# Performance work log

Measured on AMD Instinct MI355X. Metric: run time of the kernel, lower is better.

The kernel has to match this reference:

```python
import jax, jax.numpy as jnp
import numpy as np

B, S = 8, 128
D_SENS, D_ACT, D_STR, D_ENC, DIM = 512, 32, 128, 128, 128
D_JOINT = D_STR + D_ENC  # 256


def _l2norm(x):
    return x / jnp.clip(jnp.linalg.norm(x, axis=-1, keepdims=True), 1e-12)


def _mlp(x, layers):
    # layers: list of (W, b); ReLU between layers, none on output
    n = len(layers)
    for i, (W, b) in enumerate(layers):
        x = x @ W + b
        if i < n - 1:
            x = jax.nn.relu(x)
    return x


def _meta_mlp(x, p):
    x = jax.nn.relu(x @ p['W1'] + p['b1'])
    x = jax.nn.relu(x @ p['W2'] + p['b2'])
    return x @ p['W3'] + p['b3']


def setup_inputs() -> dict:
    key = jax.random.key(0)
    it = iter(jax.random.split(key, 40))
    w = lambda shape, s=0.02: jax.random.normal(next(it), shape, jnp.float32) * s
    H = D_ACT * 4  # to_transitions hidden dim (default mlp_hidden_dim)
    return dict(
        sensory=jax.random.normal(next(it), (B, S, D_SENS), jnp.float32),
        actions=jax.random.normal(next(it), (B, S, D_ACT), jnp.float32),
        init_hidden=w((1, D_STR), 0.01),
        tW1=w((D_ACT, H)), tb1=w((H,)),
        tW2=w((H, H)), tb2=w((H,)),
        tW3=w((H, D_STR * D_STR)), tb3=w((D_STR * D_STR,)),
        enc_w=w((D_SENS, D_ENC)), enc_b=w((D_ENC,)),
        dec_w=w((D_ENC, D_SENS)), dec_b=w((D_SENS,)),
        q_w=w((D_JOINT, DIM)), k_w=w((D_JOINT, DIM)), v_w=w((D_JOINT, DIM)),
        mW1=w((DIM, 2 * DIM)), mb1=w((2 * DIM,)),
        mW2=w((2 * DIM, 2 * DIM)), mb2=w((2 * DIM,)),
        mW3=w((2 * DIM, DIM)), mb3=w((DIM,)),
        oW1=w((DIM, 2 * DIM)), ob1=w((2 * DIM,)),
        oW2=w((2 * DIM, 2 * DIM)), ob2=w((2 * DIM,)),
        oW3=w((2 * DIM, D_JOINT)), ob3=w((D_JOINT,)),
        sW1=w((2 * D_STR + 1, 2 * D_STR)), sb1=w((2 * D_STR,)),
        sW2=w((2 * D_STR, 2 * D_STR)), sb2=w((2 * D_STR,)),
        sW3=w((2 * D_STR, D_STR)), sb3=w((D_STR,)),
        integration_ratio=jnp.asarray(0.1, jnp.float32),
    )


def reference(sensory, actions, init_hidden, tW1, tb1, tW2, tb2, tW3, tb3,
              enc_w, enc_b, dec_w, dec_b, q_w, k_w, v_w,
              mW1, mb1, mW2, mb2, mW3, mb3,
              oW1, ob1, oW2, ob2, oW3, ob3,
              sW1, sb1, sW2, sb2, sW3, sb3, integration_ratio):
    mse = lambda a, b: jnp.mean((a - b) ** 2)

    # --- PathIntegration: actions -> transitions -> scripted RNN scan ---
    trans = _mlp(actions, [(tW1, tb1), (tW2, tb2), (tW3, tb3)])  # (B,S,ds*ds)
    trans = trans.reshape(B, S, D_STR, D_STR)
    h0 = jnp.broadcast_to(_l2norm(init_hidden), (B, D_STR))

    def step(h, T):  # h (B,ds), T (B,ds,ds)
        h = _l2norm(jax.nn.relu(jnp.einsum('bi,bij->bj', h, T)))
        return h, h

    _, hs = jax.lax.scan(step, h0, jnp.swapaxes(trans, 0, 1))
    structural = jnp.swapaxes(hs, 0, 1)  # (B,S,ds)

    # --- sensory encoder (Linear) ---
    encoded = sensory @ enc_w + enc_b  # (B,S,D_ENC)

    meta_params = {'W1': mW1, 'b1': mb1, 'W2': mW2, 'b2': mb2, 'W3': mW3, 'b3': mb3}

    def retrieve(s, e):
        joint = jnp.concatenate((s, e), axis=-1)
        q = joint @ q_w
        r = _meta_mlp(q, meta_params)
        out = _mlp(r, [(oW1, ob1), (oW2, ob2), (oW3, ob3)])
        return out[..., :D_STR], out[..., D_STR:]

    # generative branch
    dec_gen_s, dec_enc = retrieve(structural, jnp.zeros_like(encoded))
    generative_pred_loss = mse(sensory, dec_enc @ dec_w + dec_b)

    # relational branch (source calls retrieve(zeros, encoded) twice)
    dec_s1, _ = retrieve(jnp.zeros_like(structural), encoded)
    dec_s2, _ = retrieve(jnp.zeros_like(structural), encoded)
    relational_loss = mse(dec_s1, structural) + mse(dec_s2, structural)

    # consistency / inference correction
    corr_s, corr_e = retrieve(dec_gen_s, encoded)
    sse = jnp.sum((corr_e - encoded) ** 2, axis=-1, keepdims=True)  # (B,S,1)
    pred_var = _mlp(jnp.concatenate((corr_s, dec_gen_s, sse), axis=-1),
                    [(sW1, sb1), (sW2, sb2), (sW3, sb3)])
    inf_s = dec_gen_s + (corr_s - dec_gen_s) * integration_ratio * pred_var
    consistency_loss = mse(dec_gen_s, inf_s)

    final_s, inf_e = retrieve(inf_s, jnp.zeros_like(encoded))
    inference_pred_loss = mse(sensory, inf_e @ dec_w + dec_b)

    # per-sample fast-weight memory gradients (nested vmap(grad))
    store = jnp.concatenate((final_s, encoded), axis=-1)
    keys = store @ k_w
    values = store @ v_w

    def meta_loss(p, k, v):
        return jnp.mean((_meta_mlp(k, p) - v) ** 2)

    per_grad = jax.vmap(jax.vmap(jax.grad(meta_loss), in_axes=(None, 0, 0)),
                        in_axes=(None, 0, 0))
    g = per_grad(meta_params, keys, values)  # each leaf (B,S,*param_shape)

    total = (generative_pred_loss + relational_loss
             + consistency_loss + inference_pred_loss)  # all loss weights 1.0
    return (total, g['W1'], g['b1'], g['W2'], g['b2'], g['W3'], g['b3'])
```

## Files before the change

### kernel.cpp

```cpp
#include <hip/hip_runtime.h>
#include <hip/hip_bf16.h>

constexpr size_t OFF_W1 = 1;
constexpr size_t OFF_B1 = OFF_W1 + (size_t)1024*32768;
constexpr size_t OFF_W2 = OFF_B1 + (size_t)1024*256;
constexpr size_t OFF_B2 = OFF_W2 + (size_t)1024*65536;
constexpr size_t OFF_W3 = OFF_B2 + (size_t)1024*256;
constexpr size_t OFF_B3 = OFF_W3 + (size_t)1024*32768;

__global__ __launch_bounds__(256) void gemm_kernel(
    const float* __restrict__ A, int lda,
    const float* __restrict__ W, int ldw,
    const float* __restrict__ bias,
    float* __restrict__ C, int ldc,
    int N, int K, int do_relu)
{
    __shared__ float As[16][65];
    __shared__ float Ws[16][65];
    const int tid = threadIdx.x;
    const int tx = tid & 15, ty = tid >> 4;
    const int m0 = blockIdx.x * 64, n0 = blockIdx.y * 64;
    float acc[4][4] = {};
    for (int k0 = 0; k0 < K; k0 += 16) {
        for (int l = tid; l < 1024; l += 256) {
            int mm = l >> 4, kk = l & 15;
            int gk = k0 + kk;
            As[kk][mm] = (gk < K) ? A[(size_t)(m0+mm)*lda + gk] : 0.f;
        }
        for (int l = tid; l < 1024; l += 256) {
            int kk = l >> 6, nn = l & 63;
            int gk = k0 + kk, gn = n0 + nn;
            Ws[kk][nn] = (gk < K && gn < N) ? W[(size_t)gk*ldw + gn] : 0.f;
        }
        __syncthreads();
        #pragma unroll
        for (int kk = 0; kk < 16; ++kk) {
            float a[4], b[4];
            #pragma unroll
            for (int i=0;i<4;i++) a[i] = As[kk][ty*4+i];
            #pragma unroll
            for (int j=0;j<4;j++) b[j] = Ws[kk][tx*4+j];
            #pragma unroll
            for (int i=0;i<4;i++)
                #pragma unroll
                for (int j=0;j<4;j++)
                    acc[i][j] = fmaf(a[i], b[j], acc[i][j]);
        }
        __syncthreads();
    }
    #pragma unroll
    for (int i=0;i<4;i++){
        int gm = m0 + ty*4 + i;
        #pragma unroll
        for (int j=0;j<4;j++){
            int gn = n0 + tx*4 + j;
            if (gn < N) {
                float v = acc[i][j] + (bias ? bias[gn] : 0.f);
                if (do_relu) v = fmaxf(v, 0.f);
                C[(size_t)gm*ldc + gn] = v;
            }
        }
    }
}

__global__ __launch_bounds__(256) void prep_kernel(
    const float* __restrict__ tW3,
    const float* __restrict__ mW2, const float* __restrict__ mW3,
    float* __restrict__ tW3T,
    float* __restrict__ T2, float* __restrict__ T3,
    float* __restrict__ acc)
{
    __shared__ float tile[64*129];
    const int t = threadIdx.x;
    const int bid = blockIdx.x;
    if (bid < 256) {
        const int k = bid >> 1, i0 = (bid & 1) * 64;
        const size_t base = (size_t)k << 14;
        for (int l = t; l < 8192; l += 256) {
            int ii = l >> 7, jj = l & 127;
            tile[ii*129 + jj] = tW3[base + (size_t)(i0+ii)*128 + jj];
        }
        __syncthreads();
        for (int l = t; l < 8192; l += 256) {
            int jj = l >> 6, ii = l & 63;
            tW3T[base + (size_t)jj*128 + i0 + ii] = tile[ii*129 + jj];
        }
    } else if (bid < 512) {
        const int c = bid - 256;
        T2[(size_t)c*256 + t] = mW2[(size_t)t*256 + c];
    } else if (bid < 640) {
        const int c = bid - 512;
        T3[(size_t)c*256 + t] = mW3[(size_t)t*128 + c];
    } else {
        if (t < 16) acc[t] = 0.f;
    }
}

__device__ __forceinline__ void gemm_k128_compute(
    const float* __restrict__ A, int lda, const float* __restrict__ W,
    const float* __restrict__ bias, int bias_mode, int N, int m0, int n0, int t,
    float* __restrict__ As, float4* __restrict__ acc)
{
    for (int l = t; l < 4096; l += 256) {
        int r = l >> 7, k = l & 127;
        As[k*36 + r] = A[(size_t)(m0 + r)*lda + k];
    }
    __syncthreads();
    const int c4 = (t & 63) * 4;
    const int r0 = (t >> 6) * 8;
    float4 bv;
    if (bias_mode == 0) {
        bv = *(const float4*)&bias[n0 + c4];
    } else {
        const int n = n0 + c4;
        const int j = n >> 7, i = n & 127;
        bv.x = bias[(size_t)(i+0)*128 + j];
        bv.y = bias[(size_t)(i+1)*128 + j];
        bv.z = bias[(size_t)(i+2)*128 + j];
        bv.w = bias[(size_t)(i+3)*128 + j];
    }
    #pragma unroll
    for (int i = 0; i < 8; ++i) acc[i] = bv;
    const float* Wp = W + (size_t)n0 + c4;
    #pragma unroll 4
    for (int k = 0; k < 128; ++k) {
        float4 w = *(const float4*)&Wp[(size_t)k*N];
        float a[8];
        *(float4*)&a[0] = *(const float4*)&As[k*36 + r0];
        *(float4*)&a[4] = *(const float4*)&As[k*36 + r0 + 4];
        #pragma unroll
        for (int i = 0; i < 8; ++i) {
            acc[i].x = fmaf(w.x, a[i], acc[i].x);
            acc[i].y = fmaf(w.y, a[i], acc[i].y);
            acc[i].z = fmaf(w.z, a[i], acc[i].z);
            acc[i].w = fmaf(w.w, a[i], acc[i].w);
        }
    }
}

__global__ __launch_bounds__(256) void gemm_k128_kernel(
    const float* __restrict__ A, int lda, const float* __restrict__ W,
    const float* __restrict__ bias, int bias_mode, float* __restrict__ C, int N)
{
    __shared__ float As[128*36];
    float4 acc[8];
    const int t = threadIdx.x;
    const int m0 = blockIdx.x * 32, n0 = blockIdx.y * 256;
    gemm_k128_compute(A, lda, W, bias, bias_mode, N, m0, n0, t, As, acc);
    const int c4 = (t & 63) * 4;
    const int r0 = (t >> 6) * 8;
    #pragma unroll
    for (int i = 0; i < 8; ++i)
        *(float4*)&C[(size_t)(m0 + r0 + i)*N + n0 + c4] = acc[i];
}

__global__ __launch_bounds__(256) void gemm_k128_mse_kernel(
    const float* __restrict__ A, int lda, const float* __restrict__ W,
    const float* __restrict__ bias, const float* __restrict__ ref, int N,
    float scale, float* __restrict__ accum)
{
    __shared__ float As[128*36];
    float4 acc[8];
    const int t = threadIdx.x;
    const int m0 = blockIdx.x * 32, n0 = blockIdx.y * 256;
    gemm_k128_compute(A, lda, W, bias, 0, N, m0, n0, t, As, acc);
    const int c4 = (t & 63) * 4;
    const int r0 = (t >> 6) * 8;
    float s = 0.f;
    #pragma unroll
    for (int i = 0; i < 8; ++i) {
        float4 rv = *(const float4*)&ref[(size_t)(m0 + r0 + i)*N + n0 + c4];
        float dx = acc[i].x - rv.x, dy = acc[i].y - rv.y;
        float dz = acc[i].z - rv.z, dw = acc[i].w - rv.w;
        s += dx*dx + dy*dy + dz*dz + dw*dw;
    }
    #pragma unroll
    for (int off = 32; off > 0; off >>= 1) s += __shfl_down(s, off, 64);
    __shared__ float wred[4];
    if ((t & 63) == 0) wred[t >> 6] = s;
    __syncthreads();
    if (t == 0) atomicAdd(accum, (wred[0]+wred[1]+wred[2]+wred[3]) * scale);
}

__global__ __launch_bounds__(512) void scan_kernel3(
    const float* __restrict__ transT,
    const float* __restrict__ init_hidden,
    float* __restrict__ structural)
{
    __shared__ float h[128];
    __shared__ float ws[8];
    const int b = blockIdx.x, tid = threadIdx.x;
    const int j = tid >> 2, p = tid & 3;
    const int i0 = p * 32;

    if (tid < 32) {
        float4 v = *(const float4*)&init_hidden[tid*4];
        float ss = v.x*v.x + v.y*v.y + v.z*v.z + v.w*v.w;
        ss += __shfl_xor(ss, 16); ss += __shfl_xor(ss, 8); ss += __shfl_xor(ss, 4);
        ss += __shfl_xor(ss, 2);  ss += __shfl_xor(ss, 1);
        float inv = 1.f / fmaxf(sqrtf(ss), 1e-12f);
        v.x *= inv; v.y *= inv; v.z *= inv; v.w *= inv;
        *(float4*)&h[tid*4] = v;
    }
    __syncthreads();

    const size_t bbase = ((size_t)b) << 21;
    const int lane_off = j*128 + i0;
    float4 cur[8], nxt[8];
    {
        const float* T0 = transT + bbase + lane_off;
        #pragma unroll
        for (int r = 0; r < 8; ++r) cur[r] = *(const float4*)&T0[r*4];
    }
    for (int t = 0; t < 128; ++t) {
        const int tn = (t < 127) ? t + 1 : 127;
        const float* Tn = transT + bbase + ((size_t)tn << 14) + lane_off;
        #pragma unroll
        for (int r = 0; r < 8; ++r) nxt[r] = *(const float4*)&Tn[r*4];

        float4 a = make_float4(0.f, 0.f, 0.f, 0.f);
        #pragma unroll
        for (int r = 0; r < 8; ++r) {
            float4 hv = *(const float4*)&h[i0 + r*4];
            a.x = fmaf(hv.x, cur[r].x, a.x);
            a.y = fmaf(hv.y, cur[r].y, a.y);
            a.z = fmaf(hv.z, cur[r].z, a.z);
            a.w = fmaf(hv.w, cur[r].w, a.w);
        }
        float s = (a.x + a.y) + (a.z + a.w);
        s += __shfl_xor(s, 1);
        s += __shfl_xor(s, 2);
        float v = fmaxf(s, 0.f);
        float q = v * v;
        q += __shfl_xor(q, 4);  q += __shfl_xor(q, 8);
        q += __shfl_xor(q, 16); q += __shfl_xor(q, 32);
        if ((tid & 63) == 0) ws[tid >> 6] = q;
        __syncthreads();
        float ss = ((ws[0]+ws[1]) + (ws[2]+ws[3])) + ((ws[4]+ws[5]) + (ws[6]+ws[7]));
        float inv = 1.f / fmaxf(sqrtf(ss), 1e-12f);
        float hv = v * inv;
        __syncthreads();
        if (p == 0) h[j] = hv;
        else if (p == 1) structural[(((size_t)(b*128 + t)) << 7) + j] = hv;
        __syncthreads();
        #pragma unroll
        for (int r = 0; r < 8; ++r) cur[r] = nxt[r];
    }
}

__device__ __forceinline__ void stage_rows(float* buf, const float* src, int ld,
                                           int row0, int rows, int t)
{
    int r = t >> 5; if (rows == 4) r &= 3;
    const int k4 = (t & 31) * 4;
    float4 v = make_float4(0.f,0.f,0.f,0.f);
    if (src) v = *(const float4*)&src[(size_t)(row0 + r)*ld + k4];
    *(float4*)&buf[r*128 + k4] = v;
}

__device__ __forceinline__ void layer_n256_r8(
    const float* __restrict__ W, const float* __restrict__ bias, int K,
    const float* __restrict__ x, int xs, float* __restrict__ y, int relu, int t)
{
    const int c4 = (t & 63) * 4;
    const int r0 = (t >> 6) * 2;
    float4 a0 = bias ? *(const float4*)&bias[c4] : make_float4(0.f,0.f,0.f,0.f);
    float4 a1 = a0;
    const float* x0 = x + r0 * xs;
    const float* x1 = x0 + xs;
    for (int k = 0; k < K; ++k) {
        float4 w = *(const float4*)&W[(size_t)k*256 + c4];
        float xa = x0[k], xb = x1[k];
        a0.x = fmaf(w.x, xa, a0.x); a0.y = fmaf(w.y, xa, a0.y);
        a0.z = fmaf(w.z, xa, a0.z); a0.w = fmaf(w.w, xa, a0.w);
        a1.x = fmaf(w.x, xb, a1.x); a1.y = fmaf(w.y, xb, a1.y);
        a1.z = fmaf(w.z, xb, a1.z); a1.w = fmaf(w.w, xb, a1.w);
    }
    if (relu) {
        a0.x=fmaxf(a0.x,0.f); a0.y=fmaxf(a0.y,0.f); a0.z=fmaxf(a0.z,0.f); a0.w=fmaxf(a0.w,0.f);
        a1.x=fmaxf(a1.x,0.f); a1.y=fmaxf(a1.y,0.f); a1.z=fmaxf(a1.z,0.f); a1.w=fmaxf(a1.w,0.f);
    }
    *(float4*)&y[r0*256 + c4] = a0;
    *(float4*)&y[(r0+1)*256 + c4] = a1;
}

__device__ __forceinline__ void layer_n256_r4(
    const float* __restrict__ W, const float* __restrict__ bias, int K,
    const float* __restrict__ x, int xs, float* __restrict__ y, int relu,
    const float* __restrict__ mask, int t)
{
    const int c4 = (t & 63) * 4;
    const int r = t >> 6;
    float4 a = bias ? *(const float4*)&bias[c4] : make_float4(0.f,0.f,0.f,0.f);
    const float* xr = x + r * xs;
    for (int k = 0; k < K; ++k) {
        float4 w = *(const float4*)&W[(size_t)k*256 + c4];
        float xa = xr[k];
        a.x = fmaf(w.x, xa, a.x); a.y = fmaf(w.y, xa, a.y);
        a.z = fmaf(w.z, xa, a.z); a.w = fmaf(w.w, xa, a.w);
    }
    if (relu) {
        a.x=fmaxf(a.x,0.f); a.y=fmaxf(a.y,0.f); a.z=fmaxf(a.z,0.f); a.w=fmaxf(a.w,0.f);
    }
    if (mask) {
        float4 m = *(const float4*)&mask[r*256 + c4];
        a.x = (m.x > 0.f) ? a.x : 0.f; a.y = (m.y > 0.f) ? a.y : 0.f;
        a.z = (m.z > 0.f) ? a.z : 0.f; a.w = (m.w > 0.f) ? a.w : 0.f;
    }
    *(float4*)&y[r*256 + c4] = a;
}

__device__ __forceinline__ void layer_n128(
    const float* __restrict__ W, const float* __restrict__ bias, int K,
    const float* __restrict__ x, int xs, float* __restrict__ y, int ys, int relu,
    int rows, int t)
{
    const int c4 = (t & 31) * 4;
    int r = t >> 5; if (rows == 4) r &= 3;
    float4 a = bias ? *(const float4*)&bias[c4] : make_float4(0.f,0.f,0.f,0.f);
    const float* xr = x + r * xs;
    for (int k = 0; k < K; ++k) {
        float4 w = *(const float4*)&W[(size_t)k*128 + c4];
        float xa = xr[k];
        a.x = fmaf(w.x, xa, a.x); a.y = fmaf(w.y, xa, a.y);
        a.z = fmaf(w.z, xa, a.z); a.w = fmaf(w.w, xa, a.w);
    }
    if (relu) {
        a.x=fmaxf(a.x,0.f); a.y=fmaxf(a.y,0.f); a.z=fmaxf(a.z,0.f); a.w=fmaxf(a.w,0.f);
    }
    *(float4*)&y[r*ys + c4] = a;
}

__device__ __forceinline__ void layer_n128_dual(
    const float* __restrict__ W,
    const float* __restrict__ xA, const float* __restrict__ xB,
    float* __restrict__ y, int rows, int t)
{
    const int c4 = (t & 31) * 4;
    int r = t >> 5; if (rows == 4) r &= 3;
    float4 a = make_float4(0.f,0.f,0.f,0.f);
    const float* xa_ = xA + r * 128;
    const float* xb_ = xB + r * 128;
    for (int k = 0; k < 128; ++k) {
        float4 w = *(const float4*)&W[(size_t)k*128 + c4];
        float v = xa_[k];
        a.x = fmaf(w.x, v, a.x); a.y = fmaf(w.y, v, a.y);
        a.z = fmaf(w.z, v, a.z); a.w = fmaf(w.w, v, a.w);
    }
    for (int k = 0; k < 128; ++k) {
        float4 w = *(const float4*)&W[(size_t)(128+k)*128 + c4];
        float v = xb_[k];
        a.x = fmaf(w.x, v, a.x); a.y = fmaf(w.y, v, a.y);
        a.z = fmaf(w.z, v, a.z); a.w = fmaf(w.w, v, a.w);
    }
    *(float4*)&y[r*128 + c4] = a;
}

__global__ __launch_bounds__(256) void fused_retrieve2_kernel(
    const float* __restrict__ A1a, int ld1a, const float* __restrict__ A2a, int ld2a,
    float* __restrict__ outa,
    const float* __restrict__ A1b, int ld1b, const float* __restrict__ A2b, int ld2b,
    float* __restrict__ outb,
    const float* __restrict__ qw,
    const float* __restrict__ mW1, const float* __restrict__ mb1,
    const float* __restrict__ mW2, const float* __restrict__ mb2,
    const float* __restrict__ mW3, const float* __restrict__ mb3,
    const float* __restrict__ oW1, const float* __restrict__ ob1,
    const float* __restrict__ oW2, const float* __restrict__ ob2,
    const float* __restrict__ oW3, const float* __restrict__ ob3)
{
    __shared__ float bufA[8*128], bufB[8*128], ping[8*256], pong[8*256];
    const int t = threadIdx.x;
    const bool second = blockIdx.x >= 128;
    const int row0 = (blockIdx.x & 127) * 8;
    const float* A1 = second ? A1b : A1a;  const int ld1 = second ? ld1b : ld1a;
    const float* A2 = second ? A2b : A2a;  const int ld2 = second ? ld2b : ld2a;
    float* outB = second ? outb : outa;

    stage_rows(bufA, A1, ld1, row0, 8, t);
    stage_rows(bufB, A2, ld2, row0, 8, t);
    __syncthreads();
    layer_n128_dual(qw, bufA, bufB, ping, 8, t);
    __syncthreads();
    layer_n256_r8(mW1, mb1, 128, ping, 128, pong, 1, t);
    __syncthreads();
    layer_n256_r8(mW2, mb2, 256, pong, 256, ping, 1, t);
    __syncthreads();
    layer_n128(mW3, mb3, 256, ping, 256, pong, 128, 0, 8, t);
    __syncthreads();
    layer_n256_r8(oW1, ob1, 128, pong, 128, ping, 1, t);
    __syncthreads();
    layer_n256_r8(oW2, ob2, 256, ping, 256, pong, 1, t);
    __syncthreads();
    layer_n256_r8(oW3, ob3, 256, pong, 256, ping, 0, t);
    __syncthreads();
    #pragma unroll
    for (int e = t; e < 512; e += 256) {
        int r = e >> 6, c = (e & 63) * 4;
        *(float4*)&outB[(size_t)(row0+r)*256 + c] = *(const float4*)&ping[r*256 + c];
    }
}

__global__ __launch_bounds__(256) void fused_retrieve4_kernel(
    const float* __restrict__ A1, int ld1,
    const float* __restrict__ A2, int ld2,
    const float* __restrict__ qw,
    const float* __restrict__ mW1, const float* __restrict__ mb1,
    const float* __restrict__ mW2, const float* __restrict__ mb2,
    const float* __restrict__ mW3, const float* __restrict__ mb3,
    const float* __restrict__ oW1, const float* __restrict__ ob1,
    const float* __restrict__ oW2, const float* __restrict__ ob2,
    const float* __restrict__ oW3, const float* __restrict__ ob3,
    float* __restrict__ outB)
{
    __shared__ float bufA[4*128], bufB[4*128], ping[4*256], pong[4*256];
    const int t = threadIdx.x;
    const int row0 = blockIdx.x * 4;

    stage_rows(bufA, A1, ld1, row0, 4, t);
    stage_rows(bufB, A2, ld2, row0, 4, t);
    __syncthreads();
    layer_n128_dual(qw, bufA, bufB, ping, 4, t);
    __syncthreads();
    layer_n256_r4(mW1, mb1, 128, ping, 128, pong, 1, nullptr, t);
    __syncthreads();
    layer_n256_r4(mW2, mb2, 256, pong, 256, ping, 1, nullptr, t);
    __syncthreads();
    layer_n128(mW3, mb3, 256, ping, 256, pong, 128, 0, 4, t);
    __syncthreads();
    layer_n256_r4(oW1, ob1, 128, pong, 128, ping, 1, nullptr, t);
    __syncthreads();
    layer_n256_r4(oW2, ob2, 256, ping, 256, pong, 1, nullptr, t);
    __syncthreads();
    layer_n256_r4(oW3, ob3, 256, pong, 256, ping, 0, nullptr, t);
    __syncthreads();
    {
        int r = t >> 6, c = (t & 63) * 4;
        *(float4*)&outB[(size_t)(row0+r)*256 + c] = *(const float4*)&ping[r*256 + c];
    }
}

__global__ __launch_bounds__(256) void fused_svar_kernel(
    const float* __restrict__ out3,
    const float* __restrict__ out1,
    const float* __restrict__ encoded,
    const float* __restrict__ sW1, const float* __restrict__ sb1,
    const float* __restrict__ sW2, const float* __restrict__ sb2,
    const float* __restrict__ sW3, const float* __restrict__ sb3,
    float* __restrict__ pvar)
{
    __shared__ float bufA[8*128], bufB[8*128], sse[8], ping[8*256], pong[8*256];
    const int t = threadIdx.x;
    const int row0 = blockIdx.x * 8;
    const int r = t >> 5, k4 = (t & 31) * 4;

    {
        float4 cs = *(const float4*)&out3[(size_t)(row0+r)*256 + k4];
        float4 ds = *(const float4*)&out1[(size_t)(row0+r)*256 + k4];
        *(float4*)&bufA[r*128 + k4] = cs;
        *(float4*)&bufB[r*128 + k4] = ds;
        float4 ce = *(const float4*)&out3[(size_t)(row0+r)*256 + 128 + k4];
        float4 en = *(const float4*)&encoded[(size_t)(row0+r)*128 + k4];
        float dx = ce.x-en.x, dy = ce.y-en.y, dz = ce.z-en.z, dw = ce.w-en.w;
        float ss = dx*dx + dy*dy + dz*dz + dw*dw;
        ss += __shfl_xor(ss, 16); ss += __shfl_xor(ss, 8); ss += __shfl_xor(ss, 4);
        ss += __shfl_xor(ss, 2);  ss += __shfl_xor(ss, 1);
        if ((t & 31) == 0) sse[r] = ss;
    }
    __syncthreads();
    {
        const int c4 = (t & 63) * 4;
        const int r0 = (t >> 6) * 2;
        float4 a0 = *(const float4*)&sb1[c4];
        float4 a1 = a0;
        for (int k = 0; k < 128; ++k) {
            float4 w = *(const float4*)&sW1[(size_t)k*256 + c4];
            float xa = bufA[r0*128 + k], xb = bufA[(r0+1)*128 + k];
            a0.x=fmaf(w.x,xa,a0.x); a0.y=fmaf(w.y,xa,a0.y); a0.z=fmaf(w.z,xa,a0.z); a0.w=fmaf(w.w,xa,a0.w);
            a1.x=fmaf(w.x,xb,a1.x); a1.y=fmaf(w.y,xb,a1.y); a1.z=fmaf(w.z,xb,a1.z); a1.w=fmaf(w.w,xb,a1.w);
        }
        for (int k = 0; k < 128; ++k) {
            float4 w = *(const float4*)&sW1[(size_t)(128+k)*256 + c4];
            float xa = bufB[r0*128 + k], xb = bufB[(r0+1)*128 + k];
            a0.x=fmaf(w.x,xa,a0.x); a0.y=fmaf(w.y,xa,a0.y); a0.z=fmaf(w.z,xa,a0.z); a0.w=fmaf(w.w,xa,a0.w);
            a1.x=fmaf(w.x,xb,a1.x); a1.y=fmaf(w.y,xb,a1.y); a1.z=fmaf(w.z,xb,a1.z); a1.w=fmaf(w.w,xb,a1.w);
        }
        {
            float4 w = *(const float4*)&sW1[(size_t)256*256 + c4];
            float xa = sse[r0], xb = sse[r0+1];
            a0.x=fmaf(w.x,xa,a0.x); a0.y=fmaf(w.y,xa,a0.y); a0.z=fmaf(w.z,xa,a0.z); a0.w=fmaf(w.w,xa,a0.w);
            a1.x=fmaf(w.x,xb,a1.x); a1.y=fmaf(w.y,xb,a1.y); a1.z=fmaf(w.z,xb,a1.z); a1.w=fmaf(w.w,xb,a1.w);
        }
        a0.x=fmaxf(a0.x,0.f); a0.y=fmaxf(a0.y,0.f); a0.z=fmaxf(a0.z,0.f); a0.w=fmaxf(a0.w,0.f);
        a1.x=fmaxf(a1.x,0.f); a1.y=fmaxf(a1.y,0.f); a1.z=fmaxf(a1.z,0.f); a1.w=fmaxf(a1.w,0.f);
        *(float4*)&ping[r0*256 + c4] = a0;
        *(float4*)&ping[(r0+1)*256 + c4] = a1;
    }
    __syncthreads();
    layer_n256_r8(sW2, sb2, 256, ping, 256, pong, 1, t);
    __syncthreads();
    layer_n128(sW3, sb3, 256, pong, 256, ping, 128, 0, 8, t);
    __syncthreads();
    {
        int rr = t >> 5, c = (t & 31) * 4;
        *(float4*)&pvar[(size_t)(row0+rr)*128 + c] = *(const float4*)&ping[rr*128 + c];
    }
}

__global__ __launch_bounds__(256) void fused_grad_kernel(
    const float* __restrict__ A1,
    const float* __restrict__ encoded,
    const float* __restrict__ k_w, const float* __restrict__ v_w,
    const float* __restrict__ mW1, const float* __restrict__ mb1,
    const float* __restrict__ mW2, const float* __restrict__ mb2,
    const float* __restrict__ mW3, const float* __restrict__ mb3,
    const float* __restrict__ T2,
    const float* __restrict__ T3,
    float* __restrict__ out)
{
    __shared__ float bufA[4*128], bufB[4*128], ks[4*128], vs[4*128];
    __shared__ float h1[4*256], h2[4*256], dob[4*128], dh2[4*256], dh1[4*256];
    const int t = threadIdx.x;
    const int row0 = blockIdx.x * 4;

    stage_rows(bufA, A1, 256, row0, 4, t);
    stage_rows(bufB, encoded, 128, row0, 4, t);
    __syncthreads();
    layer_n128_dual(k_w, bufA, bufB, ks, 4, t);
    layer_n128_dual(v_w, bufA, bufB, vs, 4, t);
    __syncthreads();
    layer_n256_r4(mW1, mb1, 128, ks, 128, h1, 1, nullptr, t);
    __syncthreads();
    layer_n256_r4(mW2, mb2, 256, h1, 256, h2, 1, nullptr, t);
    __syncthreads();
    layer_n128(mW3, mb3, 256, h2, 256, dob, 128, 0, 4, t);
    __syncthreads();
    for (int e = t; e < 512; e += 256)
        dob[e] = (dob[e] - vs[e]) * 0.015625f;
    __syncthreads();
    layer_n256_r4(T3, nullptr, 128, dob, 128, dh2, 0, h2, t);
    __syncthreads();
    layer_n256_r4(T2, nullptr, 256, dh2, 256, dh1, 0, h1, t);
    __syncthreads();

    #pragma unroll
    for (int r = 0; r < 4; ++r) {
        const size_t row = row0 + r;
        {
            const int c4 = (t & 63) * 4;
            const int i0 = (t >> 6) * 32;
            const float4 dv = *(const float4*)&dh1[r*256 + c4];
            float* p = out + OFF_W1 + row*32768;
            for (int i = i0; i < i0 + 32; ++i) {
                float kv = ks[r*128 + i];
                float4 o; o.x = kv*dv.x; o.y = kv*dv.y; o.z = kv*dv.z; o.w = kv*dv.w;
                *(float4*)&p[(size_t)i*256 + c4] = o;
            }
            out[OFF_B1 + row*256 + t] = dh1[r*256 + t];
        }
        {
            const int c4 = (t & 63) * 4;
            const int i0 = (t >> 6) * 64;
            const float4 dv = *(const float4*)&dh2[r*256 + c4];
            float* p = out + OFF_W2 + row*65536;
            for (int i = i0; i < i0 + 64; ++i) {
                float hv = h1[r*256 + i];
                float4 o; o.x = hv*dv.x; o.y = hv*dv.y; o.z = hv*dv.z; o.w = hv*dv.w;
                *(float4*)&p[(size_t)i*256 + c4] = o;
            }
            out[OFF_B2 + row*256 + t] = dh2[r*256 + t];
        }
        {
            const int c4 = (t & 31) * 4;
            const int i0 = (t >> 5) * 32;
            const float4 dv = *(const float4*)&dob[r*128 + c4];
            float* p = out + OFF_W3 + row*32768;
            for (int i = i0; i < i0 + 32; ++i) {
                float hv = h2[r*256 + i];
                float4 o; o.x = hv*dv.x; o.y = hv*dv.y; o.z = hv*dv.z; o.w = hv*dv.w;
                *(float4*)&p[(size_t)i*128 + c4] = o;
            }
            if (t < 128) out[OFF_B3 + row*128 + t] = dob[r*128 + t];
        }
    }
}

__global__ __launch_bounds__(256) void mse_kernel(
    const float* __restrict__ A, int lda,
    const float* __restrict__ Bm, int ldb,
    int N, float scale, float* __restrict__ accum)
{
    const int m = blockIdx.x;
    float s = 0.f;
    for (int jj = threadIdx.x; jj < N; jj += 256) {
        float d = A[(size_t)m*lda + jj] - Bm[(size_t)m*ldb + jj];
        s = fmaf(d, d, s);
    }
    #pragma unroll
    for (int off = 32; off > 0; off >>= 1) s += __shfl_down(s, off, 64);
    __shared__ float w[4];
    if ((threadIdx.x & 63) == 0) w[threadIdx.x >> 6] = s;
    __syncthreads();
    if (threadIdx.x == 0) atomicAdd(accum, (w[0]+w[1]+w[2]+w[3]) * scale);
}

__global__ __launch_bounds__(128) void infs_kernel(
    const float* __restrict__ out1,
    const float* __restrict__ out3,
    const float* __restrict__ pvar,
    const float* __restrict__ ratio_p,
    float* __restrict__ inf_s,
    float scale, float* __restrict__ accum)
{
    const int m = blockIdx.x, t = threadIdx.x;
    float ratio = ratio_p[0];
    float dgs = out1[(size_t)m*256 + t];
    float cs  = out3[(size_t)m*256 + t];
    float pv  = pvar[(size_t)m*128 + t];
    float delta = (cs - dgs) * ratio * pv;
    inf_s[(size_t)m*128 + t] = dgs + delta;
    float ss = delta * delta;
    #pragma unroll
    for (int off = 32; off > 0; off >>= 1) ss += __shfl_down(ss, off, 64);
    __shared__ float w2[2];
    if ((t & 63) == 0) w2[t >> 6] = ss;
    __syncthreads();
    if (t == 0) atomicAdd(accum, (w2[0] + w2[1]) * scale);
}

__global__ void total_kernel(const float* acc, float* out) {
    if (threadIdx.x == 0)
        out[0] = acc[0] + acc[1] + acc[2] + acc[3];
}

static inline void gemmF(const float* A, int lda, const float* W, int ldw, const float* bias,
                         float* C, int N, int K, int relu, hipStream_t s)
{
    dim3 g(16, (N + 63) / 64);
    gemm_kernel<<<g, 256, 0, s>>>(A, lda, W, ldw, bias, C, N, N, K, relu);
}

extern "C" void kernel_launch(void* const* d_in, const int* in_sizes, int n_in,
                              void* d_out, int out_size, void* d_ws, size_t ws_size,
                              hipStream_t stream)
{
    const float* sensory     = (const float*)d_in[0];
    const float* actions     = (const float*)d_in[1];
    const float* init_hidden = (const float*)d_in[2];
    const float* tW1 = (const float*)d_in[3];  const float* tb1 = (const float*)d_in[4];
    const float* tW2 = (const float*)d_in[5];  const float* tb2 = (const float*)d_in[6];
    const float* tW3 = (const float*)d_in[7];  const float* tb3 = (const float*)d_in[8];
    const float* enc_w = (const float*)d_in[9];  const float* enc_b = (const float*)d_in[10];
    const float* dec_w = (const float*)d_in[11]; const float* dec_b = (const float*)d_in[12];
    const float* q_w = (const float*)d_in[13];
    const float* k_w = (const float*)d_in[14];
    const float* v_w = (const float*)d_in[15];
    const float* mW1 = (const float*)d_in[16]; const float* mb1 = (const float*)d_in[17];
    const float* mW2 = (const float*)d_in[18]; const float* mb2 = (const float*)d_in[19];
    const float* mW3 = (const float*)d_in[20]; const float* mb3 = (const float*)d_in[21];
    const float* oW1 = (const float*)d_in[22]; const float* ob1 = (const float*)d_in[23];
    const float* oW2 = (const float*)d_in[24]; const float* ob2 = (const float*)d_in[25];
    const float* oW3 = (const float*)d_in[26]; const float* ob3 = (const float*)d_in[27];
    const float* sW1 = (const float*)d_in[28]; const float* sb1 = (const float*)d_in[29];
    const float* sW2 = (const float*)d_in[30]; const float* sb2 = (const float*)d_in[31];
    const float* sW3 = (const float*)d_in[32]; const float* sb3 = (const float*)d_in[33];
    const float* ratio = (const float*)d_in[34];
    float* out = (float*)d_out;

    float* Wsp = (float*)d_ws;
    float* acc   = Wsp;
    float* ALIAS = Wsp + 16;
    float* a1_buf     = ALIAS;
    float* structural = ALIAS + 131072;
    float* out1 = ALIAS + 262144;
    float* out2 = ALIAS + 524288;
    float* out3 = ALIAS + 786432;
    float* out4 = ALIAS + 1048576;
    float* pvar = ALIAS + 1310720;
    float* infs = ALIAS + 1441792;
    float* tW3T = ALIAS;
    size_t off = 16 + 2097152;
    float* a2      = Wsp + off; off += 131072;
    float* encoded = Wsp + off; off += 131072;
    float* transT  = Wsp + off; off += 16777216;
    float* T2      = Wsp + off; off += 65536;
    float* T3      = Wsp + off; off += 32768;

    gemmF(actions, 32, tW1, 128, tb1, a1_buf, 128, 32, 1, stream);
    gemmF(a1_buf, 128, tW2, 128, tb2, a2, 128, 128, 1, stream);

    prep_kernel<<<641, 256, 0, stream>>>(tW3, mW2, mW3, tW3T, T2, T3, acc);

    gemmF(sensory, 512, enc_w, 128, enc_b, encoded, 128, 512, 0, stream);

    gemm_k128_kernel<<<dim3(32, 64), 256, 0, stream>>>(a2, 128, tW3T, tb3, 1, transT, 16384);

    scan_kernel3<<<8, 512, 0, stream>>>(transT, init_hidden, structural);

    fused_retrieve2_kernel<<<256, 256, 0, stream>>>(
        structural, 128, nullptr, 0, out1,
        nullptr, 0, encoded, 128, out2,
        q_w, mW1, mb1, mW2, mb2, mW3, mb3, oW1, ob1, oW2, ob2, oW3, ob3);

    mse_kernel<<<1024, 256, 0, stream>>>(out2, 256, structural, 128, 128, 2.f/131072.f, acc + 1);
    gemm_k128_mse_kernel<<<dim3(32, 2), 256, 0, stream>>>(
        out1 + 128, 256, dec_w, dec_b, sensory, 512, 1.f/524288.f, acc + 0);

    fused_retrieve4_kernel<<<256, 256, 0, stream>>>(out1, 256, encoded, 128,
        q_w, mW1, mb1, mW2, mb2, mW3, mb3, oW1, ob1, oW2, ob2, oW3, ob3, out3);
    fused_svar_kernel<<<128, 256, 0, stream>>>(out3, out1, encoded,
        sW1, sb1, sW2, sb2, sW3, sb3, pvar);
    infs_kernel<<<1024, 128, 0, stream>>>(out1, out3, pvar, ratio, infs, 1.f/131072.f, acc + 2);

    fused_retrieve4_kernel<<<256, 256, 0, stream>>>(infs, 128, nullptr, 0,
        q_w, mW1, mb1, mW2, mb2, mW3, mb3, oW1, ob1, oW2, ob2, oW3, ob3, out4);
    gemm_k128_mse_kernel<<<dim3(32, 2), 256, 0, stream>>>(
        out4 + 128, 256, dec_w, dec_b, sensory, 512, 1.f/524288.f, acc + 3);

    fused_grad_kernel<<<256, 256, 0, stream>>>(out4, encoded, k_w, v_w,
        mW1, mb1, mW2, mb2, mW3, mb3, T2, T3, out);

    total_kernel<<<1, 64, 0, stream>>>(acc, out);
}
```

Baseline: 1.465 ms.

## Fuse pipeline stages into fewer kernels and overlap independent work in shared grids

Collapses the launch sequence from about fifteen kernels to six. The transition MLP and the sensory encoder are folded into the prep kernel as extra block ranges. The sequential scan is co-scheduled with the independent relational retrieval in one grid, and the decoder-MSE GEMMs ride along as extra blocks in the fused retrieve and gradient kernels. This removes launch gaps and intermediate global round-trips, and lets the 8-block scan share the GPU with other work, at the cost of heavier heterogeneous kernels with more register and shared-memory pressure.

```diff
diff --git a/kernel.cpp b/kernel.cpp
--- a/kernel.cpp
+++ b/kernel.cpp
@@ -8,92 +8,112 @@
 constexpr size_t OFF_W3 = OFF_B2 + (size_t)1024*256;
 constexpr size_t OFF_B3 = OFF_W3 + (size_t)1024*32768;
 
-__global__ __launch_bounds__(256) void gemm_kernel(
-    const float* __restrict__ A, int lda,
-    const float* __restrict__ W, int ldw,
-    const float* __restrict__ bias,
-    float* __restrict__ C, int ldc,
-    int N, int K, int do_relu)
-{
-    __shared__ float As[16][65];
-    __shared__ float Ws[16][65];
-    const int tid = threadIdx.x;
-    const int tx = tid & 15, ty = tid >> 4;
-    const int m0 = blockIdx.x * 64, n0 = blockIdx.y * 64;
-    float acc[4][4] = {};
-    for (int k0 = 0; k0 < K; k0 += 16) {
-        for (int l = tid; l < 1024; l += 256) {
-            int mm = l >> 4, kk = l & 15;
-            int gk = k0 + kk;
-            As[kk][mm] = (gk < K) ? A[(size_t)(m0+mm)*lda + gk] : 0.f;
-        }
-        for (int l = tid; l < 1024; l += 256) {
-            int kk = l >> 6, nn = l & 63;
-            int gk = k0 + kk, gn = n0 + nn;
-            Ws[kk][nn] = (gk < K && gn < N) ? W[(size_t)gk*ldw + gn] : 0.f;
-        }
-        __syncthreads();
-        #pragma unroll
-        for (int kk = 0; kk < 16; ++kk) {
-            float a[4], b[4];
-            #pragma unroll
-            for (int i=0;i<4;i++) a[i] = As[kk][ty*4+i];
-            #pragma unroll
-            for (int j=0;j<4;j++) b[j] = Ws[kk][tx*4+j];
-            #pragma unroll
-            for (int i=0;i<4;i++)
-                #pragma unroll
-                for (int j=0;j<4;j++)
-                    acc[i][j] = fmaf(a[i], b[j], acc[i][j]);
-        }
-        __syncthreads();
-    }
-    #pragma unroll
-    for (int i=0;i<4;i++){
-        int gm = m0 + ty*4 + i;
-        #pragma unroll
-        for (int j=0;j<4;j++){
-            int gn = n0 + tx*4 + j;
-            if (gn < N) {
-                float v = acc[i][j] + (bias ? bias[gn] : 0.f);
-                if (do_relu) v = fmaxf(v, 0.f);
-                C[(size_t)gm*ldc + gn] = v;
-            }
-        }
-    }
-}
-
-__global__ __launch_bounds__(256) void prep_kernel(
-    const float* __restrict__ tW3,
-    const float* __restrict__ mW2, const float* __restrict__ mW3,
-    float* __restrict__ tW3T,
-    float* __restrict__ T2, float* __restrict__ T3,
-    float* __restrict__ acc)
-{
-    __shared__ float tile[64*129];
-    const int t = threadIdx.x;
-    const int bid = blockIdx.x;
-    if (bid < 256) {
-        const int k = bid >> 1, i0 = (bid & 1) * 64;
-        const size_t base = (size_t)k << 14;
-        for (int l = t; l < 8192; l += 256) {
-            int ii = l >> 7, jj = l & 127;
-            tile[ii*129 + jj] = tW3[base + (size_t)(i0+ii)*128 + jj];
-        }
-        __syncthreads();
-        for (int l = t; l < 8192; l += 256) {
-            int jj = l >> 6, ii = l & 63;
-            tW3T[base + (size_t)jj*128 + i0 + ii] = tile[ii*129 + jj];
-        }
-    } else if (bid < 512) {
-        const int c = bid - 256;
-        T2[(size_t)c*256 + t] = mW2[(size_t)t*256 + c];
-    } else if (bid < 640) {
-        const int c = bid - 512;
-        T3[(size_t)c*256 + t] = mW3[(size_t)t*128 + c];
-    } else {
-        if (t < 16) acc[t] = 0.f;
-    }
+__device__ __forceinline__ void stage_rows(float* buf, const float* src, int ld,
+                                           int row0, int rows, int t)
+{
+    int r = t >> 5; if (rows == 4) r &= 3;
+    const int k4 = (t & 31) * 4;
+    float4 v = make_float4(0.f,0.f,0.f,0.f);
+    if (src) v = *(const float4*)&src[(size_t)(row0 + r)*ld + k4];
+    *(float4*)&buf[r*128 + k4] = v;
+}
+
+__device__ __forceinline__ void layer_n256_r8(
+    const float* __restrict__ W, const float* __restrict__ bias, int K,
+    const float* __restrict__ x, int xs, float* __restrict__ y, int relu, int t)
+{
+    const int c4 = (t & 63) * 4;
+    const int r0 = (t >> 6) * 2;
+    float4 a0 = bias ? *(const float4*)&bias[c4] : make_float4(0.f,0.f,0.f,0.f);
+    float4 a1 = a0;
+    const float* x0 = x + r0 * xs;
+    const float* x1 = x0 + xs;
+    for (int k = 0; k < K; ++k) {
+        float4 w = *(const float4*)&W[(size_t)k*256 + c4];
+        float xa = x0[k], xb = x1[k];
+        a0.x = fmaf(w.x, xa, a0.x); a0.y = fmaf(w.y, xa, a0.y);
+        a0.z = fmaf(w.z, xa, a0.z); a0.w = fmaf(w.w, xa, a0.w);
+        a1.x = fmaf(w.x, xb, a1.x); a1.y = fmaf(w.y, xb, a1.y);
+        a1.z = fmaf(w.z, xb, a1.z); a1.w = fmaf(w.w, xb, a1.w);
+    }
+    if (relu) {
+        a0.x=fmaxf(a0.x,0.f); a0.y=fmaxf(a0.y,0.f); a0.z=fmaxf(a0.z,0.f); a0.w=fmaxf(a0.w,0.f);
+        a1.x=fmaxf(a1.x,0.f); a1.y=fmaxf(a1.y,0.f); a1.z=fmaxf(a1.z,0.f); a1.w=fmaxf(a1.w,0.f);
+    }
+    *(float4*)&y[r0*256 + c4] = a0;
+    *(float4*)&y[(r0+1)*256 + c4] = a1;
+}
+
+__device__ __forceinline__ void layer_n256_r4(
+    const float* __restrict__ W, const float* __restrict__ bias, int K,
+    const float* __restrict__ x, int xs, float* __restrict__ y, int relu,
+    const float* __restrict__ mask, int t)
+{
+    const int c4 = (t & 63) * 4;
+    const int r = t >> 6;
+    float4 a = bias ? *(const float4*)&bias[c4] : make_float4(0.f,0.f,0.f,0.f);
+    const float* xr = x + r * xs;
+    for (int k = 0; k < K; ++k) {
+        float4 w = *(const float4*)&W[(size_t)k*256 + c4];
+        float xa = xr[k];
+        a.x = fmaf(w.x, xa, a.x); a.y = fmaf(w.y, xa, a.y);
+        a.z = fmaf(w.z, xa, a.z); a.w = fmaf(w.w, xa, a.w);
+    }
+    if (relu) {
+        a.x=fmaxf(a.x,0.f); a.y=fmaxf(a.y,0.f); a.z=fmaxf(a.z,0.f); a.w=fmaxf(a.w,0.f);
+    }
+    if (mask) {
+        float4 m = *(const float4*)&mask[r*256 + c4];
+        a.x = (m.x > 0.f) ? a.x : 0.f; a.y = (m.y > 0.f) ? a.y : 0.f;
+        a.z = (m.z > 0.f) ? a.z : 0.f; a.w = (m.w > 0.f) ? a.w : 0.f;
+    }
+    *(float4*)&y[r*256 + c4] = a;
+}
+
+__device__ __forceinline__ void layer_n128(
+    const float* __restrict__ W, const float* __restrict__ bias, int K,
+    const float* __restrict__ x, int xs, float* __restrict__ y, int ys, int relu,
+    int rows, int t)
+{
+    const int c4 = (t & 31) * 4;
+    int r = t >> 5; if (rows == 4) r &= 3;
+    float4 a = bias ? *(const float4*)&bias[c4] : make_float4(0.f,0.f,0.f,0.f);
+    const float* xr = x + r * xs;
+    for (int k = 0; k < K; ++k) {
+        float4 w = *(const float4*)&W[(size_t)k*128 + c4];
+        float xa = xr[k];
+        a.x = fmaf(w.x, xa, a.x); a.y = fmaf(w.y, xa, a.y);
+        a.z = fmaf(w.z, xa, a.z); a.w = fmaf(w.w, xa, a.w);
+    }
+    if (relu) {
+        a.x=fmaxf(a.x,0.f); a.y=fmaxf(a.y,0.f); a.z=fmaxf(a.z,0.f); a.w=fmaxf(a.w,0.f);
+    }
+    *(float4*)&y[r*ys + c4] = a;
+}
+
+__device__ __forceinline__ void layer_n128_dual(
+    const float* __restrict__ W,
+    const float* __restrict__ xA, const float* __restrict__ xB,
+    float* __restrict__ y, int rows, int t)
+{
+    const int c4 = (t & 31) * 4;
+    int r = t >> 5; if (rows == 4) r &= 3;
+    float4 a = make_float4(0.f,0.f,0.f,0.f);
+    const float* xa_ = xA + r * 128;
+    const float* xb_ = xB + r * 128;
+    for (int k = 0; k < 128; ++k) {
+        float4 w = *(const float4*)&W[(size_t)k*128 + c4];
+        float v = xa_[k];
+        a.x = fmaf(w.x, v, a.x); a.y = fmaf(w.y, v, a.y);
+        a.z = fmaf(w.z, v, a.z); a.w = fmaf(w.w, v, a.w);
+    }
+    for (int k = 0; k < 128; ++k) {
+        float4 w = *(const float4*)&W[(size_t)(128+k)*128 + c4];
+        float v = xb_[k];
+        a.x = fmaf(w.x, v, a.x); a.y = fmaf(w.y, v, a.y);
+        a.z = fmaf(w.z, v, a.z); a.w = fmaf(w.w, v, a.w);
+    }
+    *(float4*)&y[r*128 + c4] = a;
 }
 
 __device__ __forceinline__ void gemm_k128_compute(
@@ -154,256 +174,119 @@
         *(float4*)&C[(size_t)(m0 + r0 + i)*N + n0 + c4] = acc[i];
 }
 
-__global__ __launch_bounds__(256) void gemm_k128_mse_kernel(
-    const float* __restrict__ A, int lda, const float* __restrict__ W,
-    const float* __restrict__ bias, const float* __restrict__ ref, int N,
-    float scale, float* __restrict__ accum)
-{
-    __shared__ float As[128*36];
-    float4 acc[8];
-    const int t = threadIdx.x;
-    const int m0 = blockIdx.x * 32, n0 = blockIdx.y * 256;
-    gemm_k128_compute(A, lda, W, bias, 0, N, m0, n0, t, As, acc);
-    const int c4 = (t & 63) * 4;
-    const int r0 = (t >> 6) * 8;
-    float s = 0.f;
-    #pragma unroll
-    for (int i = 0; i < 8; ++i) {
-        float4 rv = *(const float4*)&ref[(size_t)(m0 + r0 + i)*N + n0 + c4];
-        float dx = acc[i].x - rv.x, dy = acc[i].y - rv.y;
-        float dz = acc[i].z - rv.z, dw = acc[i].w - rv.w;
-        s += dx*dx + dy*dy + dz*dz + dw*dw;
-    }
+__device__ __forceinline__ void block_mse_commit(float s, float scale,
+                                                 float* __restrict__ accum,
+                                                 float* __restrict__ red, int t)
+{
     #pragma unroll
     for (int off = 32; off > 0; off >>= 1) s += __shfl_down(s, off, 64);
-    __shared__ float wred[4];
-    if ((t & 63) == 0) wred[t >> 6] = s;
-    __syncthreads();
-    if (t == 0) atomicAdd(accum, (wred[0]+wred[1]+wred[2]+wred[3]) * scale);
-}
-
-__global__ __launch_bounds__(512) void scan_kernel3(
+    if ((t & 63) == 0) red[t >> 6] = s;
+    __syncthreads();
+    if (t == 0) atomicAdd(accum, (red[0]+red[1]+red[2]+red[3]) * scale);
+}
+
+__global__ __launch_bounds__(256) void prep_kernel(
+    const float* __restrict__ tW3,
+    const float* __restrict__ mW2, const float* __restrict__ mW3,
+    const float* __restrict__ actions,
+    const float* __restrict__ tW1, const float* __restrict__ tb1,
+    const float* __restrict__ tW2, const float* __restrict__ tb2,
+    const float* __restrict__ sensory,
+    const float* __restrict__ enc_w, const float* __restrict__ enc_b,
+    float* __restrict__ tW3T, float* __restrict__ T2, float* __restrict__ T3,
+    float* __restrict__ acc, float* __restrict__ a2, float* __restrict__ encoded)
+{
+    __shared__ float smem[64*129];
+    const int t = threadIdx.x;
+    const int bid = blockIdx.x;
+    if (bid < 256) {
+        const int k = bid >> 1, i0 = (bid & 1) * 64;
+        const size_t base = (size_t)k << 14;
+        for (int l = t; l < 8192; l += 256) {
+            int ii = l >> 7, jj = l & 127;
+            smem[ii*129 + jj] = tW3[base + (size_t)(i0+ii)*128 + jj];
+        }
+        __syncthreads();
+        for (int l = t; l < 8192; l += 256) {
+            int jj = l >> 6, ii = l & 63;
+            tW3T[base + (size_t)jj*128 + i0 + ii] = smem[ii*129 + jj];
+        }
+    } else if (bid < 512) {
+        const int c = bid - 256;
+        T2[(size_t)c*256 + t] = mW2[(size_t)t*256 + c];
+    } else if (bid < 640) {
+        const int c = bid - 512;
+        T3[(size_t)c*256 + t] = mW3[(size_t)t*128 + c];
+    } else if (bid == 640) {
+        if (t < 16) acc[t] = 0.f;
+    } else if (bid < 769) {
+        float* bufAct = smem;
+        float* ping   = smem + 256;
+        float* pong   = smem + 1280;
+        const int row0 = (bid - 641) * 8;
+        if (t < 64) {
+            int r = t >> 3, c4 = (t & 7) * 4;
+            *(float4*)&bufAct[r*32 + c4] =
+                *(const float4*)&actions[(size_t)(row0 + r)*32 + c4];
+        }
+        __syncthreads();
+        layer_n128(tW1, tb1, 32, bufAct, 32, ping, 128, 1, 8, t);
+        __syncthreads();
+        layer_n128(tW2, tb2, 128, ping, 128, pong, 128, 1, 8, t);
+        __syncthreads();
+        {
+            int r = t >> 5, c4 = (t & 31) * 4;
+            *(float4*)&a2[(size_t)(row0 + r)*128 + c4] = *(const float4*)&pong[r*128 + c4];
+        }
+    } else {
+        const int q = bid - 769;
+        const int m0 = (q & 15) * 64, n0 = (q >> 4) * 64;
+        float (*As)[65] = (float(*)[65])smem;
+        float (*Ws)[65] = (float(*)[65])(smem + 16*65);
+        const int tx = t & 15, ty = t >> 4;
+        float a4[4][4] = {};
+        for (int k0 = 0; k0 < 512; k0 += 16) {
+            for (int l = t; l < 1024; l += 256) {
+                int mm = l >> 4, kk = l & 15;
+                As[kk][mm] = sensory[(size_t)(m0+mm)*512 + k0 + kk];
+            }
+            for (int l = t; l < 1024; l += 256) {
+                int kk = l >> 6, nn = l & 63;
+                Ws[kk][nn] = enc_w[(size_t)(k0+kk)*128 + n0 + nn];
+            }
+            __syncthreads();
+            #pragma unroll
+            for (int kk = 0; kk < 16; ++kk) {
+                float a[4], b[4];
+                #pragma unroll
+                for (int i=0;i<4;i++) a[i] = As[kk][ty*4+i];
+                #pragma unroll
+                for (int j=0;j<4;j++) b[j] = Ws[kk][tx*4+j];
+                #pragma unroll
+                for (int i=0;i<4;i++)
+                    #pragma unroll
+                    for (int j=0;j<4;j++)
+                        a4[i][j] = fmaf(a[i], b[j], a4[i][j]);
+            }
+            __syncthreads();
+        }
+        #pragma unroll
+        for (int i=0;i<4;i++){
+            int gm = m0 + ty*4 + i;
+            #pragma unroll
+            for (int j=0;j<4;j++){
+                int gn = n0 + tx*4 + j;
+                encoded[(size_t)gm*128 + gn] = a4[i][j] + enc_b[gn];
+            }
+        }
+    }
+}
+
+__global__ __launch_bounds__(512) void scanrel_kernel(
     const float* __restrict__ transT,
     const float* __restrict__ init_hidden,
-    float* __restrict__ structural)
-{
-    __shared__ float h[128];
-    __shared__ float ws[8];
-    const int b = blockIdx.x, tid = threadIdx.x;
-    const int j = tid >> 2, p = tid & 3;
-    const int i0 = p * 32;
-
-    if (tid < 32) {
-        float4 v = *(const float4*)&init_hidden[tid*4];
-        float ss = v.x*v.x + v.y*v.y + v.z*v.z + v.w*v.w;
-        ss += __shfl_xor(ss, 16); ss += __shfl_xor(ss, 8); ss += __shfl_xor(ss, 4);
-        ss += __shfl_xor(ss, 2);  ss += __shfl_xor(ss, 1);
-        float inv = 1.f / fmaxf(sqrtf(ss), 1e-12f);
-        v.x *= inv; v.y *= inv; v.z *= inv; v.w *= inv;
-        *(float4*)&h[tid*4] = v;
-    }
-    __syncthreads();
-
-    const size_t bbase = ((size_t)b) << 21;
-    const int lane_off = j*128 + i0;
-    float4 cur[8], nxt[8];
-    {
-        const float* T0 = transT + bbase + lane_off;
-        #pragma unroll
-        for (int r = 0; r < 8; ++r) cur[r] = *(const float4*)&T0[r*4];
-    }
-    for (int t = 0; t < 128; ++t) {
-        const int tn = (t < 127) ? t + 1 : 127;
-        const float* Tn = transT + bbase + ((size_t)tn << 14) + lane_off;
-        #pragma unroll
-        for (int r = 0; r < 8; ++r) nxt[r] = *(const float4*)&Tn[r*4];
-
-        float4 a = make_float4(0.f, 0.f, 0.f, 0.f);
-        #pragma unroll
-        for (int r = 0; r < 8; ++r) {
-            float4 hv = *(const float4*)&h[i0 + r*4];
-            a.x = fmaf(hv.x, cur[r].x, a.x);
-            a.y = fmaf(hv.y, cur[r].y, a.y);
-            a.z = fmaf(hv.z, cur[r].z, a.z);
-            a.w = fmaf(hv.w, cur[r].w, a.w);
-        }
-        float s = (a.x + a.y) + (a.z + a.w);
-        s += __shfl_xor(s, 1);
-        s += __shfl_xor(s, 2);
-        float v = fmaxf(s, 0.f);
-        float q = v * v;
-        q += __shfl_xor(q, 4);  q += __shfl_xor(q, 8);
-        q += __shfl_xor(q, 16); q += __shfl_xor(q, 32);
-        if ((tid & 63) == 0) ws[tid >> 6] = q;
-        __syncthreads();
-        float ss = ((ws[0]+ws[1]) + (ws[2]+ws[3])) + ((ws[4]+ws[5]) + (ws[6]+ws[7]));
-        float inv = 1.f / fmaxf(sqrtf(ss), 1e-12f);
-        float hv = v * inv;
-        __syncthreads();
-        if (p == 0) h[j] = hv;
-        else if (p == 1) structural[(((size_t)(b*128 + t)) << 7) + j] = hv;
-        __syncthreads();
-        #pragma unroll
-        for (int r = 0; r < 8; ++r) cur[r] = nxt[r];
-    }
-}
-
-__device__ __forceinline__ void stage_rows(float* buf, const float* src, int ld,
-                                           int row0, int rows, int t)
-{
-    int r = t >> 5; if (rows == 4) r &= 3;
-    const int k4 = (t & 31) * 4;
-    float4 v = make_float4(0.f,0.f,0.f,0.f);
-    if (src) v = *(const float4*)&src[(size_t)(row0 + r)*ld + k4];
-    *(float4*)&buf[r*128 + k4] = v;
-}
-
-__device__ __forceinline__ void layer_n256_r8(
-    const float* __restrict__ W, const float* __restrict__ bias, int K,
-    const float* __restrict__ x, int xs, float* __restrict__ y, int relu, int t)
-{
-    const int c4 = (t & 63) * 4;
-    const int r0 = (t >> 6) * 2;
-    float4 a0 = bias ? *(const float4*)&bias[c4] : make_float4(0.f,0.f,0.f,0.f);
-    float4 a1 = a0;
-    const float* x0 = x + r0 * xs;
-    const float* x1 = x0 + xs;
-    for (int k = 0; k < K; ++k) {
-        float4 w = *(const float4*)&W[(size_t)k*256 + c4];
-        float xa = x0[k], xb = x1[k];
-        a0.x = fmaf(w.x, xa, a0.x); a0.y = fmaf(w.y, xa, a0.y);
-        a0.z = fmaf(w.z, xa, a0.z); a0.w = fmaf(w.w, xa, a0.w);
-        a1.x = fmaf(w.x, xb, a1.x); a1.y = fmaf(w.y, xb, a1.y);
-        a1.z = fmaf(w.z, xb, a1.z); a1.w = fmaf(w.w, xb, a1.w);
-    }
-    if (relu) {
-        a0.x=fmaxf(a0.x,0.f); a0.y=fmaxf(a0.y,0.f); a0.z=fmaxf(a0.z,0.f); a0.w=fmaxf(a0.w,0.f);
-        a1.x=fmaxf(a1.x,0.f); a1.y=fmaxf(a1.y,0.f); a1.z=fmaxf(a1.z,0.f); a1.w=fmaxf(a1.w,0.f);
-    }
-    *(float4*)&y[r0*256 + c4] = a0;
-    *(float4*)&y[(r0+1)*256 + c4] = a1;
-}
-
-__device__ __forceinline__ void layer_n256_r4(
-    const float* __restrict__ W, const float* __restrict__ bias, int K,
-    const float* __restrict__ x, int xs, float* __restrict__ y, int relu,
-    const float* __restrict__ mask, int t)
-{
-    const int c4 = (t & 63) * 4;
-    const int r = t >> 6;
-    float4 a = bias ? *(const float4*)&bias[c4] : make_float4(0.f,0.f,0.f,0.f);
-    const float* xr = x + r * xs;
-    for (int k = 0; k < K; ++k) {
-        float4 w = *(const float4*)&W[(size_t)k*256 + c4];
-        float xa = xr[k];
-        a.x = fmaf(w.x, xa, a.x); a.y = fmaf(w.y, xa, a.y);
-        a.z = fmaf(w.z, xa, a.z); a.w = fmaf(w.w, xa, a.w);
-    }
-    if (relu) {
-        a.x=fmaxf(a.x,0.f); a.y=fmaxf(a.y,0.f); a.z=fmaxf(a.z,0.f); a.w=fmaxf(a.w,0.f);
-    }
-    if (mask) {
-        float4 m = *(const float4*)&mask[r*256 + c4];
-        a.x = (m.x > 0.f) ? a.x : 0.f; a.y = (m.y > 0.f) ? a.y : 0.f;
-        a.z = (m.z > 0.f) ? a.z : 0.f; a.w = (m.w > 0.f) ? a.w : 0.f;
-    }
-    *(float4*)&y[r*256 + c4] = a;
-}
-
-__device__ __forceinline__ void layer_n128(
-    const float* __restrict__ W, const float* __restrict__ bias, int K,
-    const float* __restrict__ x, int xs, float* __restrict__ y, int ys, int relu,
-    int rows, int t)
-{
-    const int c4 = (t & 31) * 4;
-    int r = t >> 5; if (rows == 4) r &= 3;
-    float4 a = bias ? *(const float4*)&bias[c4] : make_float4(0.f,0.f,0.f,0.f);
-    const float* xr = x + r * xs;
-    for (int k = 0; k < K; ++k) {
-        float4 w = *(const float4*)&W[(size_t)k*128 + c4];
-        float xa = xr[k];
-        a.x = fmaf(w.x, xa, a.x); a.y = fmaf(w.y, xa, a.y);
-        a.z = fmaf(w.z, xa, a.z); a.w = fmaf(w.w, xa, a.w);
-    }
-    if (relu) {
-        a.x=fmaxf(a.x,0.f); a.y=fmaxf(a.y,0.f); a.z=fmaxf(a.z,0.f); a.w=fmaxf(a.w,0.f);
-    }
-    *(float4*)&y[r*ys + c4] = a;
-}
-
-__device__ __forceinline__ void layer_n128_dual(
-    const float* __restrict__ W,
-    const float* __restrict__ xA, const float* __restrict__ xB,
-    float* __restrict__ y, int rows, int t)
-{
-    const int c4 = (t & 31) * 4;
-    int r = t >> 5; if (rows == 4) r &= 3;
-    float4 a = make_float4(0.f,0.f,0.f,0.f);
-    const float* xa_ = xA + r * 128;
-    const float* xb_ = xB + r * 128;
-    for (int k = 0; k < 128; ++k) {
-        float4 w = *(const float4*)&W[(size_t)k*128 + c4];
-        float v = xa_[k];
-        a.x = fmaf(w.x, v, a.x); a.y = fmaf(w.y, v, a.y);
-        a.z = fmaf(w.z, v, a.z); a.w = fmaf(w.w, v, a.w);
-    }
-    for (int k = 0; k < 128; ++k) {
-        float4 w = *(const float4*)&W[(size_t)(128+k)*128 + c4];
-        float v = xb_[k];
-        a.x = fmaf(w.x, v, a.x); a.y = fmaf(w.y, v, a.y);
-        a.z = fmaf(w.z, v, a.z); a.w = fmaf(w.w, v, a.w);
-    }
-    *(float4*)&y[r*128 + c4] = a;
-}
-
-__global__ __launch_bounds__(256) void fused_retrieve2_kernel(
-    const float* __restrict__ A1a, int ld1a, const float* __restrict__ A2a, int ld2a,
-    float* __restrict__ outa,
-    const float* __restrict__ A1b, int ld1b, const float* __restrict__ A2b, int ld2b,
-    float* __restrict__ outb,
-    const float* __restrict__ qw,
-    const float* __restrict__ mW1, const float* __restrict__ mb1,
-    const float* __restrict__ mW2, const float* __restrict__ mb2,
-    const float* __restrict__ mW3, const float* __restrict__ mb3,
-    const float* __restrict__ oW1, const float* __restrict__ ob1,
-    const float* __restrict__ oW2, const float* __restrict__ ob2,
-    const float* __restrict__ oW3, const float* __restrict__ ob3)
-{
-    __shared__ float bufA[8*128], bufB[8*128], ping[8*256], pong[8*256];
-    const int t = threadIdx.x;
-    const bool second = blockIdx.x >= 128;
-    const int row0 = (blockIdx.x & 127) * 8;
-    const float* A1 = second ? A1b : A1a;  const int ld1 = second ? ld1b : ld1a;
-    const float* A2 = second ? A2b : A2a;  const int ld2 = second ? ld2b : ld2a;
-    float* outB = second ? outb : outa;
-
-    stage_rows(bufA, A1, ld1, row0, 8, t);
-    stage_rows(bufB, A2, ld2, row0, 8, t);
-    __syncthreads();
-    layer_n128_dual(qw, bufA, bufB, ping, 8, t);
-    __syncthreads();
-    layer_n256_r8(mW1, mb1, 128, ping, 128, pong, 1, t);
-    __syncthreads();
-    layer_n256_r8(mW2, mb2, 256, pong, 256, ping, 1, t);
-    __syncthreads();
-    layer_n128(mW3, mb3, 256, ping, 256, pong, 128, 0, 8, t);
-    __syncthreads();
-    layer_n256_r8(oW1, ob1, 128, pong, 128, ping, 1, t);
-    __syncthreads();
-    layer_n256_r8(oW2, ob2, 256, ping, 256, pong, 1, t);
-    __syncthreads();
-    layer_n256_r8(oW3, ob3, 256, pong, 256, ping, 0, t);
-    __syncthreads();
-    #pragma unroll
-    for (int e = t; e < 512; e += 256) {
-        int r = e >> 6, c = (e & 63) * 4;
-        *(float4*)&outB[(size_t)(row0+r)*256 + c] = *(const float4*)&ping[r*256 + c];
-    }
-}
-
-__global__ __launch_bounds__(256) void fused_retrieve4_kernel(
-    const float* __restrict__ A1, int ld1,
-    const float* __restrict__ A2, int ld2,
+    float* __restrict__ structural,
+    const float* __restrict__ encoded,
     const float* __restrict__ qw,
     const float* __restrict__ mW1, const float* __restrict__ mb1,
     const float* __restrict__ mW2, const float* __restrict__ mb2,
@@ -411,56 +294,218 @@
     const float* __restrict__ oW1, const float* __restrict__ ob1,
     const float* __restrict__ oW2, const float* __restrict__ ob2,
     const float* __restrict__ oW3, const float* __restrict__ ob3,
-    float* __restrict__ outB)
-{
-    __shared__ float bufA[4*128], bufB[4*128], ping[4*256], pong[4*256];
+    float* __restrict__ out2)
+{
+    __shared__ float smem[5120];
+    const int tid = threadIdx.x;
+    if (blockIdx.x < 8) {
+        float* h  = smem;
+        float* ws = smem + 128;
+        const int b = blockIdx.x;
+        const int j = tid >> 2, p = tid & 3;
+        const int i0 = p * 32;
+
+        if (tid < 32) {
+            float4 v = *(const float4*)&init_hidden[tid*4];
+            float ss = v.x*v.x + v.y*v.y + v.z*v.z + v.w*v.w;
+            ss += __shfl_xor(ss, 16); ss += __shfl_xor(ss, 8); ss += __shfl_xor(ss, 4);
+            ss += __shfl_xor(ss, 2);  ss += __shfl_xor(ss, 1);
+            float inv = 1.f / fmaxf(sqrtf(ss), 1e-12f);
+            v.x *= inv; v.y *= inv; v.z *= inv; v.w *= inv;
+            *(float4*)&h[tid*4] = v;
+        }
+        __syncthreads();
+
+        const size_t bbase = ((size_t)b) << 21;
+        const int lane_off = j*128 + i0;
+        float4 cur[8], nxt[8];
+        {
+            const float* T0 = transT + bbase + lane_off;
+            #pragma unroll
+            for (int r = 0; r < 8; ++r) cur[r] = *(const float4*)&T0[r*4];
+        }
+        for (int t = 0; t < 128; ++t) {
+            const int tn = (t < 127) ? t + 1 : 127;
+            const float* Tn = transT + bbase + ((size_t)tn << 14) + lane_off;
+            #pragma unroll
+            for (int r = 0; r < 8; ++r) nxt[r] = *(const float4*)&Tn[r*4];
+
+            float4 a = make_float4(0.f, 0.f, 0.f, 0.f);
+            #pragma unroll
+            for (int r = 0; r < 8; ++r) {
+                float4 hv = *(const float4*)&h[i0 + r*4];
+                a.x = fmaf(hv.x, cur[r].x, a.x);
+                a.y = fmaf(hv.y, cur[r].y, a.y);
+                a.z = fmaf(hv.z, cur[r].z, a.z);
+                a.w = fmaf(hv.w, cur[r].w, a.w);
+            }
+            float s = (a.x + a.y) + (a.z + a.w);
+            s += __shfl_xor(s, 1);
+            s += __shfl_xor(s, 2);
+            float v = fmaxf(s, 0.f);
+            float q = v * v;
+            q += __shfl_xor(q, 4);  q += __shfl_xor(q, 8);
+            q += __shfl_xor(q, 16); q += __shfl_xor(q, 32);
+            if ((tid & 63) == 0) ws[tid >> 6] = q;
+            __syncthreads();
+            float ss = ((ws[0]+ws[1]) + (ws[2]+ws[3])) + ((ws[4]+ws[5]) + (ws[6]+ws[7]));
+            float inv = 1.f / fmaxf(sqrtf(ss), 1e-12f);
+            float hv = v * inv;
+            __syncthreads();
+            if (p == 0) h[j] = hv;
+            else if (p == 1) structural[(((size_t)(b*128 + t)) << 7) + j] = hv;
+            __syncthreads();
+            #pragma unroll
+            for (int r = 0; r < 8; ++r) cur[r] = nxt[r];
+        }
+    } else {
+        float* bufB = smem;
+        float* ping = smem + 1024;
+        float* pong = smem + 3072;
+        const int row0 = (blockIdx.x - 8) * 8;
+        const bool act = (tid < 256);
+        const int t = tid;
+        if (act) stage_rows(bufB, encoded, 128, row0, 8, t);
+        __syncthreads();
+        if (act) layer_n128(qw + (size_t)128*128, nullptr, 128, bufB, 128, ping, 128, 0, 8, t);
+        __syncthreads();
+        if (act) layer_n256_r8(mW1, mb1, 128, ping, 128, pong, 1, t);
+        __syncthreads();
+        if (act) layer_n256_r8(mW2, mb2, 256, pong, 256, ping, 1, t);
+        __syncthreads();
+        if (act) layer_n128(mW3, mb3, 256, ping, 256, pong, 128, 0, 8, t);
+        __syncthreads();
+        if (act) layer_n256_r8(oW1, ob1, 128, pong, 128, ping, 1, t);
+        __syncthreads();
+        if (act) layer_n256_r8(oW2, ob2, 256, ping, 256, pong, 1, t);
+        __syncthreads();
+        if (act) layer_n256_r8(oW3, ob3, 256, pong, 256, ping, 0, t);
+        __syncthreads();
+        if (act) {
+            for (int e = t; e < 512; e += 256) {
+                int r = e >> 6, c = (e & 63) * 4;
+                *(float4*)&out2[(size_t)(row0+r)*256 + c] = *(const float4*)&ping[r*256 + c];
+            }
+        }
+    }
+}
+
+__global__ __launch_bounds__(256) void genmse_kernel(
+    const float* __restrict__ structural,
+    const float* __restrict__ qw,
+    const float* __restrict__ mW1, const float* __restrict__ mb1,
+    const float* __restrict__ mW2, const float* __restrict__ mb2,
+    const float* __restrict__ mW3, const float* __restrict__ mb3,
+    const float* __restrict__ oW1, const float* __restrict__ ob1,
+    const float* __restrict__ oW2, const float* __restrict__ ob2,
+    const float* __restrict__ oW3, const float* __restrict__ ob3,
+    float* __restrict__ out1,
+    const float* __restrict__ out2,
+    float* __restrict__ acc)
+{
+    __shared__ float smem[5120];
     const int t = threadIdx.x;
-    const int row0 = blockIdx.x * 4;
-
-    stage_rows(bufA, A1, ld1, row0, 4, t);
-    stage_rows(bufB, A2, ld2, row0, 4, t);
-    __syncthreads();
-    layer_n128_dual(qw, bufA, bufB, ping, 4, t);
-    __syncthreads();
-    layer_n256_r4(mW1, mb1, 128, ping, 128, pong, 1, nullptr, t);
-    __syncthreads();
-    layer_n256_r4(mW2, mb2, 256, pong, 256, ping, 1, nullptr, t);
-    __syncthreads();
-    layer_n128(mW3, mb3, 256, ping, 256, pong, 128, 0, 4, t);
-    __syncthreads();
-    layer_n256_r4(oW1, ob1, 128, pong, 128, ping, 1, nullptr, t);
-    __syncthreads();
-    layer_n256_r4(oW2, ob2, 256, ping, 256, pong, 1, nullptr, t);
-    __syncthreads();
-    layer_n256_r4(oW3, ob3, 256, pong, 256, ping, 0, nullptr, t);
-    __syncthreads();
-    {
-        int r = t >> 6, c = (t & 63) * 4;
-        *(float4*)&outB[(size_t)(row0+r)*256 + c] = *(const float4*)&ping[r*256 + c];
-    }
-}
-
-__global__ __launch_bounds__(256) void fused_svar_kernel(
-    const float* __restrict__ out3,
-    const float* __restrict__ out1,
-    const float* __restrict__ encoded,
+    if (blockIdx.x < 128) {
+        float* bufA = smem;
+        float* ping = smem + 1024;
+        float* pong = smem + 3072;
+        const int row0 = blockIdx.x * 8;
+        stage_rows(bufA, structural, 128, row0, 8, t);
+        __syncthreads();
+        layer_n128(qw, nullptr, 128, bufA, 128, ping, 128, 0, 8, t);
+        __syncthreads();
+        layer_n256_r8(mW1, mb1, 128, ping, 128, pong, 1, t);
+        __syncthreads();
+        layer_n256_r8(mW2, mb2, 256, pong, 256, ping, 1, t);
+        __syncthreads();
+        layer_n128(mW3, mb3, 256, ping, 256, pong, 128, 0, 8, t);
+        __syncthreads();
+        layer_n256_r8(oW1, ob1, 128, pong, 128, ping, 1, t);
+        __syncthreads();
+        layer_n256_r8(oW2, ob2, 256, ping, 256, pong, 1, t);
+        __syncthreads();
+        layer_n256_r8(oW3, ob3, 256, pong, 256, ping, 0, t);
+        __syncthreads();
+        for (int e = t; e < 512; e += 256) {
+            int r = e >> 6, c = (e & 63) * 4;
+            *(float4*)&out1[(size_t)(row0+r)*256 + c] = *(const float4*)&ping[r*256 + c];
+        }
+    } else {
+        const int m = blockIdx.x - 128;
+        float s = 0.f;
+        for (int jj = t; jj < 128; jj += 256) {
+            float d = out2[(size_t)m*256 + jj] - structural[(size_t)m*128 + jj];
+            s = fmaf(d, d, s);
+        }
+        block_mse_commit(s, 2.f/131072.f, acc + 1, smem, t);
+    }
+}
+
+__global__ __launch_bounds__(256) void bigfuse_kernel(
+    const float* __restrict__ out1, const float* __restrict__ encoded,
+    const float* __restrict__ ratio_p,
+    const float* __restrict__ qw,
+    const float* __restrict__ mW1, const float* __restrict__ mb1,
+    const float* __restrict__ mW2, const float* __restrict__ mb2,
+    const float* __restrict__ mW3, const float* __restrict__ mb3,
+    const float* __restrict__ oW1, const float* __restrict__ ob1,
+    const float* __restrict__ oW2, const float* __restrict__ ob2,
+    const float* __restrict__ oW3, const float* __restrict__ ob3,
     const float* __restrict__ sW1, const float* __restrict__ sb1,
     const float* __restrict__ sW2, const float* __restrict__ sb2,
     const float* __restrict__ sW3, const float* __restrict__ sb3,
-    float* __restrict__ pvar)
-{
-    __shared__ float bufA[8*128], bufB[8*128], sse[8], ping[8*256], pong[8*256];
+    const float* __restrict__ sensory, const float* __restrict__ dec_w,
+    const float* __restrict__ dec_b,
+    float* __restrict__ out4, float* __restrict__ acc)
+{
+    __shared__ float smem[5200];
     const int t = threadIdx.x;
-    const int row0 = blockIdx.x * 8;
-    const int r = t >> 5, k4 = (t & 31) * 4;
-
+    if (blockIdx.x >= 256) {
+        const int q = blockIdx.x - 256;
+        const int m0 = (q & 31) * 32, n0 = (q >> 5) * 256;
+        float4 a4[8];
+        gemm_k128_compute(out1 + 128, 256, dec_w, dec_b, 0, 512, m0, n0, t, smem, a4);
+        const int c4 = (t & 63) * 4;
+        const int r0 = (t >> 6) * 8;
+        float s = 0.f;
+        #pragma unroll
+        for (int i = 0; i < 8; ++i) {
+            float4 rv = *(const float4*)&sensory[(size_t)(m0 + r0 + i)*512 + n0 + c4];
+            float dx = a4[i].x - rv.x, dy = a4[i].y - rv.y;
+            float dz = a4[i].z - rv.z, dw = a4[i].w - rv.w;
+            s += dx*dx + dy*dy + dz*dz + dw*dw;
+        }
+        __syncthreads();
+        block_mse_commit(s, 1.f/524288.f, acc + 0, smem, t);
+        return;
+    }
+    float* out1_s = smem;
+    float* enc_s  = smem + 512;
+    float* out3_s = smem + 1024;
+    float* ping   = smem + 2048;
+    float* pong   = smem + 3072;
+    float* pvar_s = smem + 4096;
+    float* infs_s = smem + 4608;
+    float* sse    = smem + 5120;
+    float* red    = smem + 5124;
+    const int row0 = blockIdx.x * 4;
     {
-        float4 cs = *(const float4*)&out3[(size_t)(row0+r)*256 + k4];
-        float4 ds = *(const float4*)&out1[(size_t)(row0+r)*256 + k4];
-        *(float4*)&bufA[r*128 + k4] = cs;
-        *(float4*)&bufB[r*128 + k4] = ds;
-        float4 ce = *(const float4*)&out3[(size_t)(row0+r)*256 + 128 + k4];
-        float4 en = *(const float4*)&encoded[(size_t)(row0+r)*128 + k4];
+        int r = (t >> 5) & 3, k4 = (t & 31) * 4;
+        *(float4*)&out1_s[r*128 + k4] = *(const float4*)&out1[(size_t)(row0+r)*256 + k4];
+        *(float4*)&enc_s[r*128 + k4]  = *(const float4*)&encoded[(size_t)(row0+r)*128 + k4];
+    }
+    __syncthreads();
+    layer_n128_dual(qw, out1_s, enc_s, ping, 4, t); __syncthreads();
+    layer_n256_r4(mW1, mb1, 128, ping, 128, pong, 1, nullptr, t); __syncthreads();
+    layer_n256_r4(mW2, mb2, 256, pong, 256, ping, 1, nullptr, t); __syncthreads();
+    layer_n128(mW3, mb3, 256, ping, 256, pong, 128, 0, 4, t); __syncthreads();
+    layer_n256_r4(oW1, ob1, 128, pong, 128, ping, 1, nullptr, t); __syncthreads();
+    layer_n256_r4(oW2, ob2, 256, ping, 256, pong, 1, nullptr, t); __syncthreads();
+    layer_n256_r4(oW3, ob3, 256, pong, 256, out3_s, 0, nullptr, t); __syncthreads();
+    {
+        int r = (t >> 5) & 3, k4 = (t & 31) * 4;
+        float4 ce = *(const float4*)&out3_s[r*256 + 128 + k4];
+        float4 en = *(const float4*)&enc_s[r*128 + k4];
         float dx = ce.x-en.x, dy = ce.y-en.y, dz = ce.z-en.z, dw = ce.w-en.w;
         float ss = dx*dx + dy*dy + dz*dz + dw*dw;
         ss += __shfl_xor(ss, 16); ss += __shfl_xor(ss, 8); ss += __shfl_xor(ss, 4);
@@ -470,60 +515,104 @@
     __syncthreads();
     {
         const int c4 = (t & 63) * 4;
-        const int r0 = (t >> 6) * 2;
-        float4 a0 = *(const float4*)&sb1[c4];
-        float4 a1 = a0;
+        const int r = t >> 6;
+        float4 a = *(const float4*)&sb1[c4];
         for (int k = 0; k < 128; ++k) {
             float4 w = *(const float4*)&sW1[(size_t)k*256 + c4];
-            float xa = bufA[r0*128 + k], xb = bufA[(r0+1)*128 + k];
-            a0.x=fmaf(w.x,xa,a0.x); a0.y=fmaf(w.y,xa,a0.y); a0.z=fmaf(w.z,xa,a0.z); a0.w=fmaf(w.w,xa,a0.w);
-            a1.x=fmaf(w.x,xb,a1.x); a1.y=fmaf(w.y,xb,a1.y); a1.z=fmaf(w.z,xb,a1.z); a1.w=fmaf(w.w,xb,a1.w);
+            float xa = out3_s[r*256 + k];
+            a.x=fmaf(w.x,xa,a.x); a.y=fmaf(w.y,xa,a.y); a.z=fmaf(w.z,xa,a.z); a.w=fmaf(w.w,xa,a.w);
         }
         for (int k = 0; k < 128; ++k) {
             float4 w = *(const float4*)&sW1[(size_t)(128+k)*256 + c4];
-            float xa = bufB[r0*128 + k], xb = bufB[(r0+1)*128 + k];
-            a0.x=fmaf(w.x,xa,a0.x); a0.y=fmaf(w.y,xa,a0.y); a0.z=fmaf(w.z,xa,a0.z); a0.w=fmaf(w.w,xa,a0.w);
-            a1.x=fmaf(w.x,xb,a1.x); a1.y=fmaf(w.y,xb,a1.y); a1.z=fmaf(w.z,xb,a1.z); a1.w=fmaf(w.w,xb,a1.w);
+            float xa = out1_s[r*128 + k];
+            a.x=fmaf(w.x,xa,a.x); a.y=fmaf(w.y,xa,a.y); a.z=fmaf(w.z,xa,a.z); a.w=fmaf(w.w,xa,a.w);
         }
         {
             float4 w = *(const float4*)&sW1[(size_t)256*256 + c4];
-            float xa = sse[r0], xb = sse[r0+1];
-            a0.x=fmaf(w.x,xa,a0.x); a0.y=fmaf(w.y,xa,a0.y); a0.z=fmaf(w.z,xa,a0.z); a0.w=fmaf(w.w,xa,a0.w);
-            a1.x=fmaf(w.x,xb,a1.x); a1.y=fmaf(w.y,xb,a1.y); a1.z=fmaf(w.z,xb,a1.z); a1.w=fmaf(w.w,xb,a1.w);
-        }
-        a0.x=fmaxf(a0.x,0.f); a0.y=fmaxf(a0.y,0.f); a0.z=fmaxf(a0.z,0.f); a0.w=fmaxf(a0.w,0.f);
-        a1.x=fmaxf(a1.x,0.f); a1.y=fmaxf(a1.y,0.f); a1.z=fmaxf(a1.z,0.f); a1.w=fmaxf(a1.w,0.f);
-        *(float4*)&ping[r0*256 + c4] = a0;
-        *(float4*)&ping[(r0+1)*256 + c4] = a1;
-    }
-    __syncthreads();
-    layer_n256_r8(sW2, sb2, 256, ping, 256, pong, 1, t);
-    __syncthreads();
-    layer_n128(sW3, sb3, 256, pong, 256, ping, 128, 0, 8, t);
-    __syncthreads();
+            float xa = sse[r];
+            a.x=fmaf(w.x,xa,a.x); a.y=fmaf(w.y,xa,a.y); a.z=fmaf(w.z,xa,a.z); a.w=fmaf(w.w,xa,a.w);
+        }
+        a.x=fmaxf(a.x,0.f); a.y=fmaxf(a.y,0.f); a.z=fmaxf(a.z,0.f); a.w=fmaxf(a.w,0.f);
+        *(float4*)&ping[r*256 + c4] = a;
+    }
+    __syncthreads();
+    layer_n256_r4(sW2, sb2, 256, ping, 256, pong, 1, nullptr, t); __syncthreads();
+    layer_n128(sW3, sb3, 256, pong, 256, pvar_s, 128, 0, 4, t); __syncthreads();
     {
-        int rr = t >> 5, c = (t & 31) * 4;
-        *(float4*)&pvar[(size_t)(row0+rr)*128 + c] = *(const float4*)&ping[rr*128 + c];
-    }
-}
-
-__global__ __launch_bounds__(256) void fused_grad_kernel(
-    const float* __restrict__ A1,
-    const float* __restrict__ encoded,
+        float ratio = ratio_p[0];
+        float ssum = 0.f;
+        for (int e = t; e < 512; e += 256) {
+            int r = e >> 7, j = e & 127;
+            float dgs = out1_s[r*128 + j];
+            float cs  = out3_s[r*256 + j];
+            float pv  = pvar_s[r*128 + j];
+            float delta = (cs - dgs) * ratio * pv;
+            infs_s[r*128 + j] = dgs + delta;
+            ssum = fmaf(delta, delta, ssum);
+        }
+        #pragma unroll
+        for (int off = 32; off > 0; off >>= 1) ssum += __shfl_down(ssum, off, 64);
+        if ((t & 63) == 0) red[t >> 6] = ssum;
+    }
+    __syncthreads();
+    if (t == 0) atomicAdd(acc + 2, (red[0]+red[1]+red[2]+red[3]) * (1.f/131072.f));
+    layer_n128(qw, nullptr, 128, infs_s, 128, ping, 128, 0, 4, t); __syncthreads();
+    layer_n256_r4(mW1, mb1, 128, ping, 128, pong, 1, nullptr, t); __syncthreads();
+    layer_n256_r4(mW2, mb2, 256, pong, 256, ping, 1, nullptr, t); __syncthreads();
+    layer_n128(mW3, mb3, 256, ping, 256, pong, 128, 0, 4, t); __syncthreads();
+    layer_n256_r4(oW1, ob1, 128, pong, 128, ping, 1, nullptr, t); __syncthreads();
+    layer_n256_r4(oW2, ob2, 256, ping, 256, pong, 1, nullptr, t); __syncthreads();
+    layer_n256_r4(oW3, ob3, 256, pong, 256, ping, 0, nullptr, t); __syncthreads();
+    {
+        int r = t >> 6, c4 = (t & 63) * 4;
+        *(float4*)&out4[(size_t)(row0+r)*256 + c4] = *(const float4*)&ping[r*256 + c4];
+    }
+}
+
+__global__ __launch_bounds__(256) void gradfuse_kernel(
+    const float* __restrict__ out4, const float* __restrict__ encoded,
     const float* __restrict__ k_w, const float* __restrict__ v_w,
     const float* __restrict__ mW1, const float* __restrict__ mb1,
     const float* __restrict__ mW2, const float* __restrict__ mb2,
     const float* __restrict__ mW3, const float* __restrict__ mb3,
-    const float* __restrict__ T2,
-    const float* __restrict__ T3,
-    float* __restrict__ out)
-{
-    __shared__ float bufA[4*128], bufB[4*128], ks[4*128], vs[4*128];
-    __shared__ float h1[4*256], h2[4*256], dob[4*128], dh2[4*256], dh1[4*256];
+    const float* __restrict__ T2, const float* __restrict__ T3,
+    const float* __restrict__ sensory, const float* __restrict__ dec_w,
+    const float* __restrict__ dec_b,
+    float* __restrict__ acc, float* __restrict__ out)
+{
+    __shared__ float smem[6656];
     const int t = threadIdx.x;
+    if (blockIdx.x >= 256) {
+        const int q = blockIdx.x - 256;
+        const int m0 = (q & 31) * 32, n0 = (q >> 5) * 256;
+        float4 a4[8];
+        gemm_k128_compute(out4 + 128, 256, dec_w, dec_b, 0, 512, m0, n0, t, smem, a4);
+        const int c4 = (t & 63) * 4;
+        const int r0 = (t >> 6) * 8;
+        float s = 0.f;
+        #pragma unroll
+        for (int i = 0; i < 8; ++i) {
+            float4 rv = *(const float4*)&sensory[(size_t)(m0 + r0 + i)*512 + n0 + c4];
+            float dx = a4[i].x - rv.x, dy = a4[i].y - rv.y;
+            float dz = a4[i].z - rv.z, dw = a4[i].w - rv.w;
+            s += dx*dx + dy*dy + dz*dz + dw*dw;
+        }
+        __syncthreads();
+        block_mse_commit(s, 1.f/524288.f, acc + 3, smem, t);
+        return;
+    }
+    float* bufA = smem;
+    float* bufB = smem + 512;
+    float* ks   = smem + 1024;
+    float* vs   = smem + 1536;
+    float* h1   = smem + 2048;
+    float* h2   = smem + 3072;
+    float* dob  = smem + 4096;
+    float* dh2  = smem + 4608;
+    float* dh1  = smem + 5632;
     const int row0 = blockIdx.x * 4;
 
-    stage_rows(bufA, A1, 256, row0, 4, t);
+    stage_rows(bufA, out4, 256, row0, 4, t);
     stage_rows(bufB, encoded, 128, row0, 4, t);
     __syncthreads();
     layer_n128_dual(k_w, bufA, bufB, ks, 4, t);
@@ -585,59 +674,9 @@
     }
 }
 
-__global__ __launch_bounds__(256) void mse_kernel(
-    const float* __restrict__ A, int lda,
-    const float* __restrict__ Bm, int ldb,
-    int N, float scale, float* __restrict__ accum)
-{
-    const int m = blockIdx.x;
-    float s = 0.f;
-    for (int jj = threadIdx.x; jj < N; jj += 256) {
-        float d = A[(size_t)m*lda + jj] - Bm[(size_t)m*ldb + jj];
-        s = fmaf(d, d, s);
-    }
-    #pragma unroll
-    for (int off = 32; off > 0; off >>= 1) s += __shfl_down(s, off, 64);
-    __shared__ float w[4];
-    if ((threadIdx.x & 63) == 0) w[threadIdx.x >> 6] = s;
-    __syncthreads();
-    if (threadIdx.x == 0) atomicAdd(accum, (w[0]+w[1]+w[2]+w[3]) * scale);
-}
-
-__global__ __launch_bounds__(128) void infs_kernel(
-    const float* __restrict__ out1,
-    const float* __restrict__ out3,
-    const float* __restrict__ pvar,
-    const float* __restrict__ ratio_p,
-    float* __restrict__ inf_s,
-    float scale, float* __restrict__ accum)
-{
-    const int m = blockIdx.x, t = threadIdx.x;
-    float ratio = ratio_p[0];
-    float dgs = out1[(size_t)m*256 + t];
-    float cs  = out3[(size_t)m*256 + t];
-    float pv  = pvar[(size_t)m*128 + t];
-    float delta = (cs - dgs) * ratio * pv;
-    inf_s[(size_t)m*128 + t] = dgs + delta;
-    float ss = delta * delta;
-    #pragma unroll
-    for (int off = 32; off > 0; off >>= 1) ss += __shfl_down(ss, off, 64);
-    __shared__ float w2[2];
-    if ((t & 63) == 0) w2[t >> 6] = ss;
-    __syncthreads();
-    if (t == 0) atomicAdd(accum, (w2[0] + w2[1]) * scale);
-}
-
 __global__ void total_kernel(const float* acc, float* out) {
     if (threadIdx.x == 0)
         out[0] = acc[0] + acc[1] + acc[2] + acc[3];
-}
-
-static inline void gemmF(const float* A, int lda, const float* W, int ldw, const float* bias,
-                         float* C, int N, int K, int relu, hipStream_t s)
-{
-    dim3 g(16, (N + 63) / 64);
-    gemm_kernel<<<g, 256, 0, s>>>(A, lda, W, ldw, bias, C, N, N, K, relu);
 }
 
 extern "C" void kernel_launch(void* const* d_in, const int* in_sizes, int n_in,
@@ -670,14 +709,10 @@
     float* Wsp = (float*)d_ws;
     float* acc   = Wsp;
     float* ALIAS = Wsp + 16;
-    float* a1_buf     = ALIAS;
     float* structural = ALIAS + 131072;
     float* out1 = ALIAS + 262144;
     float* out2 = ALIAS + 524288;
-    float* out3 = ALIAS + 786432;
     float* out4 = ALIAS + 1048576;
-    float* pvar = ALIAS + 1310720;
-    float* infs = ALIAS + 1441792;
     float* tW3T = ALIAS;
     size_t off = 16 + 2097152;
     float* a2      = Wsp + off; off += 131072;
@@ -686,39 +721,25 @@
     float* T2      = Wsp + off; off += 65536;
     float* T3      = Wsp + off; off += 32768;
 
-    gemmF(actions, 32, tW1, 128, tb1, a1_buf, 128, 32, 1, stream);
-    gemmF(a1_buf, 128, tW2, 128, tb2, a2, 128, 128, 1, stream);
-
-    prep_kernel<<<641, 256, 0, stream>>>(tW3, mW2, mW3, tW3T, T2, T3, acc);
-
-    gemmF(sensory, 512, enc_w, 128, enc_b, encoded, 128, 512, 0, stream);
+    prep_kernel<<<801, 256, 0, stream>>>(tW3, mW2, mW3, actions, tW1, tb1, tW2, tb2,
+                                         sensory, enc_w, enc_b, tW3T, T2, T3,
+                                         acc, a2, encoded);
 
     gemm_k128_kernel<<<dim3(32, 64), 256, 0, stream>>>(a2, 128, tW3T, tb3, 1, transT, 16384);
 
-    scan_kernel3<<<8, 512, 0, stream>>>(transT, init_hidden, structural);
-
-    fused_retrieve2_kernel<<<256, 256, 0, stream>>>(
-        structural, 128, nullptr, 0, out1,
-        nullptr, 0, encoded, 128, out2,
-        q_w, mW1, mb1, mW2, mb2, mW3, mb3, oW1, ob1, oW2, ob2, oW3, ob3);
-
-    mse_kernel<<<1024, 256, 0, stream>>>(out2, 256, structural, 128, 128, 2.f/131072.f, acc + 1);
-    gemm_k128_mse_kernel<<<dim3(32, 2), 256, 0, stream>>>(
-        out1 + 128, 256, dec_w, dec_b, sensory, 512, 1.f/524288.f, acc + 0);
-
-    fused_retrieve4_kernel<<<256, 256, 0, stream>>>(out1, 256, encoded, 128,
-        q_w, mW1, mb1, mW2, mb2, mW3, mb3, oW1, ob1, oW2, ob2, oW3, ob3, out3);
-    fused_svar_kernel<<<128, 256, 0, stream>>>(out3, out1, encoded,
-        sW1, sb1, sW2, sb2, sW3, sb3, pvar);
-    infs_kernel<<<1024, 128, 0, stream>>>(out1, out3, pvar, ratio, infs, 1.f/131072.f, acc + 2);
-
-    fused_retrieve4_kernel<<<256, 256, 0, stream>>>(infs, 128, nullptr, 0,
-        q_w, mW1, mb1, mW2, mb2, mW3, mb3, oW1, ob1, oW2, ob2, oW3, ob3, out4);
-    gemm_k128_mse_kernel<<<dim3(32, 2), 256, 0, stream>>>(
-        out4 + 128, 256, dec_w, dec_b, sensory, 512, 1.f/524288.f, acc + 3);
-
-    fused_grad_kernel<<<256, 256, 0, stream>>>(out4, encoded, k_w, v_w,
-        mW1, mb1, mW2, mb2, mW3, mb3, T2, T3, out);
+    scanrel_kernel<<<136, 512, 0, stream>>>(transT, init_hidden, structural, encoded,
+        q_w, mW1, mb1, mW2, mb2, mW3, mb3, oW1, ob1, oW2, ob2, oW3, ob3, out2);
+
+    genmse_kernel<<<1152, 256, 0, stream>>>(structural,
+        q_w, mW1, mb1, mW2, mb2, mW3, mb3, oW1, ob1, oW2, ob2, oW3, ob3,
+        out1, out2, acc);
+
+    bigfuse_kernel<<<320, 256, 0, stream>>>(out1, encoded, ratio,
+        q_w, mW1, mb1, mW2, mb2, mW3, mb3, oW1, ob1, oW2, ob2, oW3, ob3,
+        sW1, sb1, sW2, sb2, sW3, sb3, sensory, dec_w, dec_b, out4, acc);
+
+    gradfuse_kernel<<<320, 256, 0, stream>>>(out4, encoded, k_w, v_w,
+        mW1, mb1, mW2, mb2, mW3, mb3, T2, T3, sensory, dec_w, dec_b, acc, out);
 
     total_kernel<<<1, 64, 0, stream>>>(acc, out);
 }
```

Result: faster. 1.337 ms (-8.7%).
